# Kernel tuning notes

Measured on AMD Instinct MI355X. Metric: run time of the kernel, lower is better.

## Reference

```python
import jax, jax.numpy as jnp
import numpy as np

B, N, DE, DH, L, DC = 8, 256, 768, 192, 2, 192
NEG = 1e30  # mask_logic constant from the repo


def setup_inputs() -> dict:
    ks = iter(jax.random.split(jax.random.key(0), 32))

    def nrm(shape, s=0.02):
        return jax.random.normal(next(ks), shape, dtype=jnp.float32) * s

    features = jax.random.normal(next(ks), (B, N, DE), dtype=jnp.float32)
    # DAG adjacency: node i attends to a subset of j < i; guarantee edge (i, i-1)
    rnd = jax.random.bernoulli(next(ks), 0.3, (B, N, N))
    tril = jnp.tril(jnp.ones((N, N), jnp.bool_), -1)
    adj = ((rnd & tril[None]) | jnp.eye(N, k=-1, dtype=jnp.bool_)[None]).astype(jnp.float32)
    s_mask = jax.random.bernoulli(next(ks), 0.5, (B, N, N)).astype(jnp.float32)
    s_mask_onehot = jnp.stack([1.0 - s_mask, s_mask], axis=-1)  # unused in forward
    lengths = jnp.full((B,), N, dtype=jnp.int32)  # unused (nodal_att_type=None)
    return dict(
        features=features, adj=adj, s_mask=s_mask,
        s_mask_onehot=s_mask_onehot, lengths=lengths,
        fc1_w=nrm((DE, DH)), fc1_b=jnp.zeros((DH,), jnp.float32),
        gat_w=nrm((L, 2 * DH)), gat_b=jnp.zeros((L,), jnp.float32),
        wr0=nrm((L, DH, DH)), wr1=nrm((L, DH, DH)),
        gruc_wih=nrm((L, 3 * DH, DH)), gruc_whh=nrm((L, 3 * DH, DH)),
        gruc_bih=jnp.zeros((L, 3 * DH), jnp.float32),
        gruc_bhh=jnp.zeros((L, 3 * DH), jnp.float32),
        grup_wih=nrm((L, 3 * DH, DH)), grup_whh=nrm((L, 3 * DH, DH)),
        grup_bih=jnp.zeros((L, 3 * DH), jnp.float32),
        grup_bhh=jnp.zeros((L, 3 * DH), jnp.float32),
        mlp_w0=nrm((DH * (L + 1), DH)), mlp_b0=jnp.zeros((DH,), jnp.float32),
        mlp_w1=nrm((DH, DH)), mlp_b1=jnp.zeros((DH,), jnp.float32),
        mlp_w2=nrm((DH, DC)), mlp_b2=jnp.zeros((DC,), jnp.float32),
    )


def _gru(x, h, wih, whh, bih, bhh):
    # torch.nn.GRUCell math
    gi = x @ wih.T + bih
    gh = h @ whh.T + bhh
    ir, iz, inn = jnp.split(gi, 3, axis=-1)
    hr, hz, hn = jnp.split(gh, 3, axis=-1)
    r = jax.nn.sigmoid(ir + hr)
    z = jax.nn.sigmoid(iz + hz)
    n = jnp.tanh(inn + r * hn)
    return (1.0 - z) * n + z * h


def _layer(Hl, adj, s_mask, gat_w, gat_b, wr0, wr1, cw, cp):
    # One DAG layer: sequential scan over nodes. Carry holds the relation-
    # projected value buffers V0=H1@Wr0^T, V1=H1@Wr1^T and per-node key
    # scores Ksc=H1@wk (rows >= i are zero and masked out), which is
    # mathematically identical to the torch code that re-projects the
    # growing H1 every step.
    wq, wk = gat_w[:DH], gat_w[DH:]
    pos = jnp.arange(N)

    def step(carry, xs):
        V0, V1, Ksc = carry
        i, x_i, adj_i, sm_i = xs  # x_i:(B,DH) adj_i,sm_i:(B,N)
        score = (x_i @ wq)[:, None] + Ksc + gat_b          # (B,N)
        mask = (pos < i)[None, :] & (adj_i > 0.5)          # ragged :i slice
        alpha = jnp.where(mask, score, score - NEG)        # mask_logic
        attn = jax.nn.softmax(alpha, axis=-1)              # masked -> exactly 0
        Vrel = V0 * sm_i[..., None] + V1 * (1.0 - sm_i[..., None])
        M = jnp.einsum('bn,bnd->bd', attn, Vrel)
        M = jnp.where(i > 0, M, 0.0)                       # node 0: no context
        C = _gru(x_i, M, *cw)
        P = _gru(M, x_i, *cp)
        Hnew = C + P
        V0 = V0.at[:, i, :].set(Hnew @ wr0.T)
        V1 = V1.at[:, i, :].set(Hnew @ wr1.T)
        Ksc = Ksc.at[:, i].set(Hnew @ wk)
        attn_out = jnp.where(i > 0, attn, 0.0)             # adjB row 0 is zeros
        return (V0, V1, Ksc), (Hnew, attn_out)

    z3 = jnp.zeros((B, N, DH), jnp.float32)
    carry0 = (z3, z3, jnp.zeros((B, N), jnp.float32))
    xs = (pos, Hl.transpose(1, 0, 2), adj.transpose(1, 0, 2), s_mask.transpose(1, 0, 2))
    _, (Hseq, Aseq) = jax.lax.scan(step, carry0, xs)
    return Hseq.transpose(1, 0, 2), Aseq.transpose(1, 0, 2)  # (B,N,DH),(B,N,N)


def reference(features, adj, s_mask, s_mask_onehot, lengths,
              fc1_w, fc1_b, gat_w, gat_b, wr0, wr1,
              gruc_wih, gruc_whh, gruc_bih, gruc_bhh,
              grup_wih, grup_whh, grup_bih, grup_bhh,
              mlp_w0, mlp_b0, mlp_w1, mlp_b1, mlp_w2, mlp_b2):
    Hl = jax.nn.relu(features @ fc1_w + fc1_b)  # H0
    Hs, As = [Hl], []
    for l in range(L):
        cw = (gruc_wih[l], gruc_whh[l], gruc_bih[l], gruc_bhh[l])
        cp = (grup_wih[l], grup_whh[l], grup_bih[l], grup_bhh[l])
        Hl, Al = _layer(Hl, adj, s_mask, gat_w[l], gat_b[l], wr0[l], wr1[l], cw, cp)
        Hs.append(Hl)
        As.append(Al)
    H = jnp.concatenate(Hs, axis=2)  # (B,N,DH*(L+1))
    # nodal_att_type=None => attentive_node_features is identity
    h = jax.nn.relu(H @ mlp_w0 + mlp_b0)
    h = jax.nn.relu(h @ mlp_w1 + mlp_b1)  # mlp_layers-1 = 1 extra block
    logits = h @ mlp_w2 + mlp_b2          # dropout: eval-mode identity
    return logits, jnp.stack(As, axis=1)  # (B,N,DC), (B,L,N,N)
```

## Files before the change

kernel.cpp:

```cpp
#include <hip/hip_runtime.h>
#include <stdint.h>

#define B_  8
#define N_  256
#define DH_ 192
#define L_  2
#define G3  576
#define G6  1152
#define NW  4
#define DS  48
#define KD  24
#define GC  288
#define STH 10001
#define STP 20001
#define STQ 25001
#define SPK 50000
#define SF1 50001
#define SF2 50002
#define SDN 60001

typedef unsigned long long u64;

__device__ __forceinline__ float bflo(uint32_t u) { return __uint_as_float(u << 16); }
__device__ __forceinline__ float bfhi(uint32_t u) { return __uint_as_float(u & 0xffff0000u); }
__device__ __forceinline__ uint32_t f2bf(float f) {
    uint32_t x = __float_as_uint(f);
    x += 0x7fffu + ((x >> 16) & 1u);
    return x >> 16;
}
__device__ __forceinline__ float sigm(float x)  { return 1.f / (1.f + __expf(-x)); }
__device__ __forceinline__ float tanhf_(float x){ return 1.f - 2.f / (1.f + __expf(2.f * x)); }
__device__ __forceinline__ u64 packvs(float v, int st) {
    return ((u64)(uint32_t)st << 32) | __float_as_uint(v);
}
__device__ __forceinline__ u64 agload(const u64* p) {
    return __hip_atomic_load(p, __ATOMIC_RELAXED, __HIP_MEMORY_SCOPE_AGENT);
}
__device__ __forceinline__ void agstore(u64* p, u64 v) {
    __hip_atomic_store(p, v, __ATOMIC_RELAXED, __HIP_MEMORY_SCOPE_AGENT);
}

struct ScanSm {
    uint4 Wlds4[24 * GC];
    uint4 Wr4s[12 * DH_];
    float sA0[N_], sA1[N_], sKsc[N_];
    float sAdjN[N_], sSmN[N_];
    float sXq[DH_], sPre[6 * DS], sXv[DS];
    float sM[DH_], su0[DS], su1[DS], sGc[GC], sHn[DS];
    float sRedS[4], sRedX[3], sSaved[4];
};
struct WorkSm {
    uint4 Wp4[24 * GC];
    float sX[DH_];
    float sPv[GC];
    float sRed[3];
};
struct PrologSm {
    float sA[8][768];
    float sRed[3][8][192];
};
struct MlpSm {
    float sH[8][576];
    float sRed[3][8][192];
    float sT[8][192];
};

__device__ void prepack_slice(int idx,
    const float* __restrict__ wr0, const float* __restrict__ wr1,
    const float* __restrict__ c_wih, const float* __restrict__ c_whh,
    const float* __restrict__ c_bih, const float* __restrict__ c_bhh,
    const float* __restrict__ p_wih, const float* __restrict__ p_whh,
    const float* __restrict__ p_bih, const float* __restrict__ p_bhh,
    float* __restrict__ WpreT, uint32_t* __restrict__ W4,
    uint32_t* __restrict__ Wr4, uint32_t* __restrict__ Wp4w,
    float* __restrict__ biasPre, float* __restrict__ gbx)
{
    for (int l = 0; l < L_; ++l) {
        const float* cwih = c_wih + l * G3 * DH_;
        const float* cwhh = c_whh + l * G3 * DH_;
        const float* pwih = p_wih + l * G3 * DH_;
        const float* pwhh = p_whh + l * G3 * DH_;
        if (l == 0) {
            int k = idx / G6, r = idx - k * G6;
            float w = (r < G3) ? cwih[r * DH_ + k] : pwhh[(r - G3) * DH_ + k];
            WpreT[k * G6 + r] = w;
        }
        if (idx < NW * 27648) {
            int w = idx / 27648, pos = idx % 27648;
            int p4 = pos / 1152, rem = pos % 1152;
            int c2 = rem >> 2, s = rem & 3;
            int p = 4 * p4 + s;
            int j = c2 / DS, dd = c2 % DS;
            int c = 192 * j + DS * w + dd;
            float w0 = (c < G3) ? cwhh[c * DH_ + 2 * p]     : pwih[(c - G3) * DH_ + 2 * p];
            float w1 = (c < G3) ? cwhh[c * DH_ + 2 * p + 1] : pwih[(c - G3) * DH_ + 2 * p + 1];
            W4[l * NW * 27648 + idx] = f2bf(w0) | (f2bf(w1) << 16);
            if (l == 1) {
                int r = c;
                float v0 = (r < G3) ? cwih[r * DH_ + 2 * p]     : pwhh[(r - G3) * DH_ + 2 * p];
                float v1 = (r < G3) ? cwih[r * DH_ + 2 * p + 1] : pwhh[(r - G3) * DH_ + 2 * p + 1];
                Wp4w[idx] = f2bf(v0) | (f2bf(v1) << 16);
            }
        }
        if (idx < NW * 9216) {
            int w = idx / 9216, pos = idx % 9216;
            int kq = pos / 768, rem = pos % 768;
            int d = rem >> 2, s = rem & 3;
            int k = DS * w + 4 * kq + s;
            Wr4[l * NW * 9216 + idx] =
                f2bf(wr0[l * DH_ * DH_ + d * DH_ + k]) |
                (f2bf(wr1[l * DH_ * DH_ + d * DH_ + k]) << 16);
        }
        if (idx < G6) {
            float base = (idx < G3) ? c_bih[l * G3 + idx] : p_bhh[l * G3 + idx - G3];
            float fold = 0.f;
            if (idx < 384)                    fold = c_bhh[l * G3 + idx];
            else if (idx >= G3 && idx < 960)  fold = p_bih[l * G3 + idx - G3];
            biasPre[l * G6 + idx] = base + fold;
        }
        if (idx < 384) {
            gbx[l * 384 + idx] = (idx < DH_) ? c_bhh[l * G3 + 384 + idx]
                                             : p_bih[l * G3 + 384 + (idx - DH_)];
        }
    }
}

__device__ void flag_sync(u64* flags, int wgid, int t, int stamp)
{
    __threadfence();
    __syncthreads();
    if (t == 0) agstore(&flags[wgid], packvs(0.f, stamp));
    if (t < 96) {
        while ((uint32_t)(agload(&flags[t]) >> 32) != (uint32_t)stamp) {}
    }
    __syncthreads();
    __threadfence();
    __syncthreads();
}

__device__ void prologue(char* smem, int wgid, int t,
    const float* __restrict__ features, const float* __restrict__ fc1_w,
    const float* __restrict__ fc1_b, const float* __restrict__ WpreT,
    const float* __restrict__ biasPre,
    float* __restrict__ Hcat, float* __restrict__ PREg, u64* __restrict__ Fp)
{
    PrologSm* P = (PrologSm*)smem;
    const int c = t % 192, kg = t / 192;
    for (int tt = wgid; tt < 256; tt += 96) {
        const int r0 = tt * 8;
        for (int q = t; q < 1536; q += 576) {
            int r = q / 192, c4 = q % 192;
            *(float4*)&P->sA[r][4 * c4] = *(const float4*)(features + (size_t)(r0 + r) * 768 + 4 * c4);
        }
        __syncthreads();
        {
            const float* bp = fc1_w + (size_t)(kg * 256) * 192 + c;
            float acc[8] = {0.f, 0.f, 0.f, 0.f, 0.f, 0.f, 0.f, 0.f};
            #pragma unroll 8
            for (int kk = 0; kk < 256; ++kk) {
                float bv = bp[(size_t)kk * 192];
                #pragma unroll
                for (int rr = 0; rr < 8; ++rr) acc[rr] += P->sA[rr][kg * 256 + kk] * bv;
            }
            #pragma unroll
            for (int rr = 0; rr < 8; ++rr) P->sRed[kg][rr][c] = acc[rr];
        }
        __syncthreads();
        if (t < 192) {
            float bv = fc1_b[t];
            #pragma unroll
            for (int rr = 0; rr < 8; ++rr) {
                float v = P->sRed[0][rr][t] + P->sRed[1][rr][t] + P->sRed[2][rr][t] + bv;
                Hcat[(size_t)(r0 + rr) * G3 + t] = fmaxf(v, 0.f);
            }
        }
        __syncthreads();
    }
    flag_sync(Fp + 96, wgid, t, SF1);
    {
        const float bpa = biasPre[t], bpb = biasPre[576 + t];
        for (int tt = wgid; tt < 256; tt += 96) {
            const int r0 = tt * 8;
            for (int q = t; q < 384; q += 576) {
                int r = q / 48, c4 = q % 48;
                *(float4*)&P->sA[r][4 * c4] = *(const float4*)(Hcat + (size_t)(r0 + r) * G3 + 4 * c4);
            }
            __syncthreads();
            {
                const float* b0 = WpreT + t;
                float a0[8] = {0.f,0.f,0.f,0.f,0.f,0.f,0.f,0.f};
                float a1[8] = {0.f,0.f,0.f,0.f,0.f,0.f,0.f,0.f};
                #pragma unroll 4
                for (int k = 0; k < 192; ++k) {
                    float bva = b0[(size_t)k * G6];
                    float bvb = b0[(size_t)k * G6 + 576];
                    #pragma unroll
                    for (int rr = 0; rr < 8; ++rr) {
                        float av = P->sA[rr][k];
                        a0[rr] += av * bva; a1[rr] += av * bvb;
                    }
                }
                #pragma unroll
                for (int rr = 0; rr < 8; ++rr) {
                    PREg[(size_t)(r0 + rr) * G6 + t]       = a0[rr] + bpa;
                    PREg[(size_t)(r0 + rr) * G6 + 576 + t] = a1[rr] + bpb;
                }
            }
            __syncthreads();
        }
    }
    flag_sync(Fp + 192, wgid, t, SF2);
}

__device__ void mlp_tail(char* smem, int wgid, int t,
    const float* __restrict__ Hcat,
    const float* __restrict__ mw0, const float* __restrict__ mb0,
    const float* __restrict__ mw1, const float* __restrict__ mb1,
    const float* __restrict__ mw2, const float* __restrict__ mb2,
    float* __restrict__ out, u64* __restrict__ Fd)
{
    if (t < 64) {
        while ((uint32_t)(agload(&Fd[t]) >> 32) != (uint32_t)SDN) {}
    }
    __syncthreads();
    __threadfence();
    __syncthreads();
    MlpSm* M = (MlpSm*)smem;
    const int c = t % 192, kg = t / 192;
    for (int tt = wgid; tt < 256; tt += 96) {
        const int r0 = tt * 8;
        for (int q = t; q < 1152; q += 576) {
            int r = q / 144, c4 = q % 144;
            *(float4*)&M->sH[r][4 * c4] = *(const float4*)(Hcat + (size_t)(r0 + r) * G3 + 4 * c4);
        }
        __syncthreads();
        {
            const float* bp = mw0 + (size_t)(kg * 192) * 192 + c;
            float acc[8] = {0.f,0.f,0.f,0.f,0.f,0.f,0.f,0.f};
            #pragma unroll 8
            for (int kk = 0; kk < 192; ++kk) {
                float bv = bp[(size_t)kk * 192];
                #pragma unroll
                for (int rr = 0; rr < 8; ++rr) acc[rr] += M->sH[rr][kg * 192 + kk] * bv;
            }
            #pragma unroll
            for (int rr = 0; rr < 8; ++rr) M->sRed[kg][rr][c] = acc[rr];
        }
        __syncthreads();
        if (t < 192) {
            float bv = mb0[t];
            #pragma unroll
            for (int rr = 0; rr < 8; ++rr)
                M->sT[rr][t] = fmaxf(M->sRed[0][rr][t] + M->sRed[1][rr][t] + M->sRed[2][rr][t] + bv, 0.f);
        }
        __syncthreads();
        {
            const float* bp = mw1 + (size_t)(kg * 64) * 192 + c;
            float acc[8] = {0.f,0.f,0.f,0.f,0.f,0.f,0.f,0.f};
            #pragma unroll 8
            for (int kk = 0; kk < 64; ++kk) {
                float bv = bp[(size_t)kk * 192];
                #pragma unroll
                for (int rr = 0; rr < 8; ++rr) acc[rr] += M->sT[rr][kg * 64 + kk] * bv;
            }
            #pragma unroll
            for (int rr = 0; rr < 8; ++rr) M->sRed[kg][rr][c] = acc[rr];
        }
        __syncthreads();
        if (t < 192) {
            float bv = mb1[t];
            #pragma unroll
            for (int rr = 0; rr < 8; ++rr)
                M->sH[rr][t] = fmaxf(M->sRed[0][rr][t] + M->sRed[1][rr][t] + M->sRed[2][rr][t] + bv, 0.f);
        }
        __syncthreads();
        {
            const float* bp = mw2 + (size_t)(kg * 64) * 192 + c;
            float acc[8] = {0.f,0.f,0.f,0.f,0.f,0.f,0.f,0.f};
            #pragma unroll 8
            for (int kk = 0; kk < 64; ++kk) {
                float bv = bp[(size_t)kk * 192];
                #pragma unroll
                for (int rr = 0; rr < 8; ++rr) acc[rr] += M->sH[rr][kg * 64 + kk] * bv;
            }
            #pragma unroll
            for (int rr = 0; rr < 8; ++rr) M->sRed[kg][rr][c] = acc[rr];
        }
        __syncthreads();
        if (t < 192) {
            float bv = mb2[t];
            #pragma unroll
            for (int rr = 0; rr < 8; ++rr)
                out[(size_t)(r0 + rr) * 192 + t] =
                    M->sRed[0][rr][t] + M->sRed[1][rr][t] + M->sRed[2][rr][t] + bv;
        }
        __syncthreads();
    }
}

template<int ISL2>
__device__ void scan_body(
    ScanSm* S, int b, int w, int t,
    const float* __restrict__ xin, float* __restrict__ hout,
    const float* __restrict__ PREg, const float* __restrict__ adj,
    const float* __restrict__ smask,
    const uint32_t* __restrict__ W4l, const uint32_t* __restrict__ Wr4l,
    const float* __restrict__ gbxl, const float* __restrict__ gatwl,
    uint32_t* __restrict__ Hw, u64* __restrict__ MPsl, u64* __restrict__ Kdl,
    u64* __restrict__ HcW, const u64* __restrict__ HcR,
    const u64* __restrict__ PREcR, const u64* __restrict__ XQcR,
    float* __restrict__ AsB, int sbase)
{
    const int lane = t & 63, wave = t >> 6;
    const int dg0 = w * DS;
    const float* adjB = adj   + (size_t)b * N_ * N_;
    const float* smB  = smask + (size_t)b * N_ * N_;
    const int fi = b * NW;

    {
        uint32_t* wl = (uint32_t*)S->Wlds4;
        for (int q = t; q < 27648; q += 576) wl[q] = W4l[q];
        uint32_t* wr = (uint32_t*)S->Wr4s;
        for (int q = t; q < 9216; q += 576) wr[q] = Wr4l[q];
    }
    float wqv = (!ISL2 && t < DH_) ? gatwl[t] : 0.f;
    float wkv = 0.f, g2b = 0.f, g5b = 0.f;
    if (t < DS) { wkv = gatwl[DH_ + dg0 + t]; g2b = gbxl[dg0 + t]; g5b = gbxl[DH_ + dg0 + t]; }
    if (t < N_) S->sKsc[t] = 0.f;
    if (w == 0 && t < N_) AsB[t] = 0.f;

    if (!ISL2) {
        if (t < DS) {
            const float* pre = PREg + (size_t)(b * N_) * G6 + dg0 + t;
            S->sPre[t] = pre[0]; S->sPre[DS + t] = pre[192]; S->sPre[2 * DS + t] = pre[384];
            S->sPre[3 * DS + t] = pre[576]; S->sPre[4 * DS + t] = pre[768]; S->sPre[5 * DS + t] = pre[960];
            S->sXv[t] = xin[(size_t)(b * N_) * G3 + dg0 + t];
        }
        for (int q = t; q < 176; q += 576) {
            if (q < 64)       *(float4*)&S->sAdjN[4 * q] = *(const float4*)(adjB + N_ + 4 * q);
            else if (q < 128) { int q2 = q - 64;  *(float4*)&S->sSmN[4 * q2] = *(const float4*)(smB + N_ + 4 * q2); }
            else              { int q2 = q - 128; *(float4*)&S->sXq[4 * q2] = *(const float4*)(xin + (size_t)(b * N_ + 1) * G3 + 4 * q2); }
        }
    } else {
        for (int q = t; q < 321; q += 576) {
            if (q < 64)       *(float4*)&S->sAdjN[4 * q] = *(const float4*)(adjB + N_ + 4 * q);
            else if (q < 128) { int q2 = q - 64;  *(float4*)&S->sSmN[4 * q2] = *(const float4*)(smB + N_ + 4 * q2); }
            else if (q < 176) {
                int d = q - 128;
                const u64* p = HcR + ((size_t)(b * N_) * NW + w) * DS + d;
                u64 v; do { v = agload(p); } while ((uint32_t)(v >> 32) != (uint32_t)STH);
                S->sXv[d] = __uint_as_float((uint32_t)v);
            } else if (q < 320) {
                int qq = q - 176;
                const u64* p = PREcR + ((size_t)(b * N_) * NW + w) * 144 + qq;
                u64 v; do { v = agload(p); } while ((uint32_t)(v >> 32) != (uint32_t)STP);
                uint32_t pl = (uint32_t)v;
                S->sPre[2 * qq] = bflo(pl); S->sPre[2 * qq + 1] = bfhi(pl);
            } else {
                const u64* p = XQcR + b * N_ + 1;
                u64 v; do { v = agload(p); } while ((uint32_t)(v >> 32) != (uint32_t)(STQ + 1));
                S->sSaved[3] = __uint_as_float((uint32_t)v);
            }
        }
    }
    __syncthreads();
    {
        float hn = 0.f;
        if (t < DS) {
            float xv = S->sXv[t];
            float r1 = sigm(S->sPre[t]), z1 = sigm(S->sPre[DS + t]);
            float n1 = tanhf_(S->sPre[2 * DS + t] + r1 * g2b);
            float Cv = (1.f - z1) * n1;
            float r2 = sigm(S->sPre[3 * DS + t]), z2 = sigm(S->sPre[4 * DS + t]);
            float n2 = tanhf_(g5b + r2 * S->sPre[5 * DS + t]);
            hn = Cv + (1.f - z2) * n2 + z2 * xv;
            S->sHn[t] = hn;
            hout[(size_t)(b * N_) * G3 + dg0 + t] = hn;
            if (!ISL2) HcW[((size_t)(b * N_) * NW + w) * DS + t] = packvs(hn, STH);
        }
        if (wave == 0) {
            float v = hn * wkv;
            #pragma unroll
            for (int o = 32; o; o >>= 1) v += __shfl_xor(v, o);
            if (lane == 0) agstore(&Kdl[fi + w], packvs(v, sbase));
        }
    }
    __syncthreads();
    if (t < KD) Hw[(size_t)t * N_] = f2bf(S->sHn[2 * t]) | (f2bf(S->sHn[2 * t + 1]) << 16);
    if (!ISL2) {
        float px = (t < DH_) ? S->sXq[t] * wqv : 0.f;
        #pragma unroll
        for (int o = 32; o; o >>= 1) px += __shfl_xor(px, o);
        if (t < DH_ && lane == 0) S->sRedX[wave] = px;
    }
    __syncthreads();
    float xq = ISL2 ? S->sSaved[3] : (S->sRedX[0] + S->sRedX[1] + S->sRedX[2]);

    for (int i = 1; i < N_; ++i) {
        const int row = b * N_ + i;
        const int stamp = sbase + i;
        {
            float e = 0.f;
            if (t == i - 1) { S->sSaved[0] = S->sAdjN[t]; S->sSaved[1] = S->sSmN[t]; }
            if (t < N_) {
                if (t < i - 1 && S->sAdjN[t] > 0.5f) e = __expf(xq + S->sKsc[t]);
                float b0 = e * S->sSmN[t];
                S->sA0[t] = b0; S->sA1[t] = e - b0;
            }
            float ps = e;
            #pragma unroll
            for (int o = 32; o; o >>= 1) ps += __shfl_xor(ps, o);
            if (t < N_ && lane == 0) S->sRedS[wave] = ps;
        }
        __syncthreads();
        if (t < 384) {
            const int ilim = i - 1;
            const int kd = t >> 4, jp = t & 15;
            const uint32_t* hp = Hw + (size_t)kd * N_;
            float u0l = 0.f, u0h = 0.f, u1l = 0.f, u1h = 0.f;
            int j = jp;
            while (j + 48 < ilim) {
                uint32_t h0 = hp[j], h1 = hp[j + 16], h2 = hp[j + 32], h3 = hp[j + 48];
                float b0, b1;
                b0 = S->sA0[j];      b1 = S->sA1[j];
                u0l = fmaf(b0, bflo(h0), u0l); u0h = fmaf(b0, bfhi(h0), u0h);
                u1l = fmaf(b1, bflo(h0), u1l); u1h = fmaf(b1, bfhi(h0), u1h);
                b0 = S->sA0[j + 16]; b1 = S->sA1[j + 16];
                u0l = fmaf(b0, bflo(h1), u0l); u0h = fmaf(b0, bfhi(h1), u0h);
                u1l = fmaf(b1, bflo(h1), u1l); u1h = fmaf(b1, bfhi(h1), u1h);
                b0 = S->sA0[j + 32]; b1 = S->sA1[j + 32];
                u0l = fmaf(b0, bflo(h2), u0l); u0h = fmaf(b0, bfhi(h2), u0h);
                u1l = fmaf(b1, bflo(h2), u1l); u1h = fmaf(b1, bfhi(h2), u1h);
                b0 = S->sA0[j + 48]; b1 = S->sA1[j + 48];
                u0l = fmaf(b0, bflo(h3), u0l); u0h = fmaf(b0, bfhi(h3), u0h);
                u1l = fmaf(b1, bflo(h3), u1l); u1h = fmaf(b1, bfhi(h3), u1h);
                j += 64;
            }
            for (; j < ilim; j += 16) {
                uint32_t hv = hp[j];
                float b0 = S->sA0[j], b1 = S->sA1[j];
                u0l = fmaf(b0, bflo(hv), u0l); u0h = fmaf(b0, bfhi(hv), u0h);
                u1l = fmaf(b1, bflo(hv), u1l); u1h = fmaf(b1, bfhi(hv), u1h);
            }
            #pragma unroll
            for (int o = 1; o <= 8; o <<= 1) {
                u0l += __shfl_xor(u0l, o); u0h += __shfl_xor(u0h, o);
                u1l += __shfl_xor(u1l, o); u1h += __shfl_xor(u1h, o);
            }
            if (jp == 0) {
                S->su0[2 * kd] = u0l; S->su0[2 * kd + 1] = u0h;
                S->su1[2 * kd] = u1l; S->su1[2 * kd + 1] = u1h;
            }
        } else {
            const int u = t - 384;
            const int inx = (i + 1 < N_) ? i + 1 : N_ - 1;
            if (!ISL2) {
                for (int q = u; q < 260; q += 192) {
                    if (q < 64)
                        *(float4*)&S->sAdjN[4 * q] = *(const float4*)(adjB + (size_t)inx * N_ + 4 * q);
                    else if (q < 128) { int q2 = q - 64;
                        *(float4*)&S->sSmN[4 * q2] = *(const float4*)(smB + (size_t)inx * N_ + 4 * q2); }
                    else if (q < 140) { int q2 = q - 128;
                        *(float4*)&S->sXv[4 * q2] = *(const float4*)(xin + (size_t)row * G3 + dg0 + 4 * q2); }
                    else if (q < 212) { int q2 = q - 140; int g = q2 / 12, o = q2 - 12 * g;
                        *(float4*)&S->sPre[g * DS + 4 * o] =
                            *(const float4*)(PREg + (size_t)row * G6 + g * DH_ + dg0 + 4 * o); }
                    else { int q2 = q - 212;
                        *(float4*)&S->sXq[4 * q2] = *(const float4*)(xin + (size_t)(b * N_ + inx) * G3 + 4 * q2); }
                }
            } else {
                for (int q = u; q < 321; q += 192) {
                    if (q < 64)
                        *(float4*)&S->sAdjN[4 * q] = *(const float4*)(adjB + (size_t)inx * N_ + 4 * q);
                    else if (q < 128) { int q2 = q - 64;
                        *(float4*)&S->sSmN[4 * q2] = *(const float4*)(smB + (size_t)inx * N_ + 4 * q2); }
                    else if (q < 176) {
                        int d = q - 128;
                        const u64* p = HcR + ((size_t)row * NW + w) * DS + d;
                        u64 v; do { v = agload(p); } while ((uint32_t)(v >> 32) != (uint32_t)(STH + i));
                        S->sXv[d] = __uint_as_float((uint32_t)v);
                    } else if (q < 320) {
                        int qq = q - 176;
                        const u64* p = PREcR + ((size_t)row * NW + w) * 144 + qq;
                        u64 v; do { v = agload(p); } while ((uint32_t)(v >> 32) != (uint32_t)(STP + i));
                        uint32_t pl = (uint32_t)v;
                        S->sPre[2 * qq] = bflo(pl); S->sPre[2 * qq + 1] = bfhi(pl);
                    } else {
                        const u64* p = XQcR + b * N_ + inx;
                        u64 v; do { v = agload(p); } while ((uint32_t)(v >> 32) != (uint32_t)(STQ + inx));
                        S->sSaved[3] = __uint_as_float((uint32_t)v);
                    }
                }
            }
            if (t == 575) {
                const uint32_t ex = (uint32_t)(stamp - 1);
                u64 k0, k1, k2, k3;
                do {
                    k0 = agload(&Kdl[fi + 0]); k1 = agload(&Kdl[fi + 1]);
                    k2 = agload(&Kdl[fi + 2]); k3 = agload(&Kdl[fi + 3]);
                } while ((uint32_t)(k0 >> 32) != ex || (uint32_t)(k1 >> 32) != ex ||
                         (uint32_t)(k2 >> 32) != ex || (uint32_t)(k3 >> 32) != ex);
                float kdot = __uint_as_float((uint32_t)k0) + __uint_as_float((uint32_t)k1)
                           + __uint_as_float((uint32_t)k2) + __uint_as_float((uint32_t)k3);
                float adjI1 = S->sSaved[0], smI1 = S->sSaved[1];
                float e1 = (adjI1 > 0.5f) ? __expf(xq + kdot) : 0.f;
                float Ssum = S->sRedS[0] + S->sRedS[1] + S->sRedS[2] + S->sRedS[3] + e1;
                S->sKsc[i - 1] = kdot;
                float c0 = e1 * smI1;
                S->sA0[i - 1] = c0; S->sA1[i - 1] = e1 - c0;
                S->sSaved[2] = 1.f / Ssum;
            }
        }
        __syncthreads();
        if (t < DH_) {
            float mp = 0.f, h0a = 0.f, h1a = 0.f;
            #pragma unroll 4
            for (int kq = 0; kq < 12; ++kq) {
                uint4 wv = S->Wr4s[kq * DH_ + t];
                const int k0 = 4 * kq;
                float lo, hi;
                lo = bflo(wv.x); hi = bfhi(wv.x);
                mp = fmaf(S->su0[k0 + 0], lo, mp); mp = fmaf(S->su1[k0 + 0], hi, mp);
                h0a = fmaf(S->sHn[k0 + 0], lo, h0a); h1a = fmaf(S->sHn[k0 + 0], hi, h1a);
                lo = bflo(wv.y); hi = bfhi(wv.y);
                mp = fmaf(S->su0[k0 + 1], lo, mp); mp = fmaf(S->su1[k0 + 1], hi, mp);
                h0a = fmaf(S->sHn[k0 + 1], lo, h0a); h1a = fmaf(S->sHn[k0 + 1], hi, h1a);
                lo = bflo(wv.z); hi = bfhi(wv.z);
                mp = fmaf(S->su0[k0 + 2], lo, mp); mp = fmaf(S->su1[k0 + 2], hi, mp);
                h0a = fmaf(S->sHn[k0 + 2], lo, h0a); h1a = fmaf(S->sHn[k0 + 2], hi, h1a);
                lo = bflo(wv.w); hi = bfhi(wv.w);
                mp = fmaf(S->su0[k0 + 3], lo, mp); mp = fmaf(S->su1[k0 + 3], hi, mp);
                h0a = fmaf(S->sHn[k0 + 3], lo, h0a); h1a = fmaf(S->sHn[k0 + 3], hi, h1a);
            }
            float invS = S->sSaved[2];
            mp = (mp + S->sA0[i - 1] * h0a + S->sA1[i - 1] * h1a) * invS;
            agstore(&MPsl[(size_t)(fi + w) * DH_ + t], packvs(mp, stamp));
            const int w1 = (w + 1) & 3, w2 = (w + 2) & 3, w3 = (w + 3) & 3;
            u64* pA = &MPsl[(size_t)(fi + w1) * DH_ + t];
            u64* pB = &MPsl[(size_t)(fi + w2) * DH_ + t];
            u64* pC = &MPsl[(size_t)(fi + w3) * DH_ + t];
            const uint32_t ex = (uint32_t)stamp;
            u64 vA, vB, vC;
            do {
                vA = agload(pA); vB = agload(pB); vC = agload(pC);
            } while ((uint32_t)(vA >> 32) != ex || (uint32_t)(vB >> 32) != ex ||
                     (uint32_t)(vC >> 32) != ex);
            S->sM[t] = mp + __uint_as_float((uint32_t)vA)
                          + __uint_as_float((uint32_t)vB)
                          + __uint_as_float((uint32_t)vC);
        } else if (w == 0 && t < 448) {
            int j = t - 192;
            AsB[(size_t)i * N_ + j] = (S->sA0[j] + S->sA1[j]) * S->sSaved[2];
        }
        __syncthreads();
        {
            const int c = t >> 1, kh = t & 1;
            const uint4* wp = S->Wlds4 + (12 * kh) * GC + c;
            float g = 0.f;
            #pragma unroll 4
            for (int p4 = 0; p4 < 12; ++p4) {
                uint4 wv = wp[p4 * GC];
                const int m0 = 8 * (12 * kh + p4);
                g = fmaf(S->sM[m0 + 0], bflo(wv.x), g); g = fmaf(S->sM[m0 + 1], bfhi(wv.x), g);
                g = fmaf(S->sM[m0 + 2], bflo(wv.y), g); g = fmaf(S->sM[m0 + 3], bfhi(wv.y), g);
                g = fmaf(S->sM[m0 + 4], bflo(wv.z), g); g = fmaf(S->sM[m0 + 5], bfhi(wv.z), g);
                g = fmaf(S->sM[m0 + 6], bflo(wv.w), g); g = fmaf(S->sM[m0 + 7], bfhi(wv.w), g);
            }
            g += __shfl_xor(g, 1);
            if (kh == 0) S->sGc[c] = g;
        }
        __syncthreads();
        {
            float hn = 0.f;
            if (t < DS) {
                float Mv = S->sM[dg0 + t];
                float r1 = sigm(S->sPre[t] + S->sGc[t]);
                float z1 = sigm(S->sPre[DS + t] + S->sGc[DS + t]);
                float n1 = tanhf_(S->sPre[2 * DS + t] + r1 * (S->sGc[2 * DS + t] + g2b));
                float Cv = (1.f - z1) * n1 + z1 * Mv;
                float r2 = sigm(S->sGc[3 * DS + t] + S->sPre[3 * DS + t]);
                float z2 = sigm(S->sGc[4 * DS + t] + S->sPre[4 * DS + t]);
                float n2 = tanhf_(S->sGc[5 * DS + t] + g5b + r2 * S->sPre[5 * DS + t]);
                hn = Cv + (1.f - z2) * n2 + z2 * S->sXv[t];
                S->sHn[t] = hn;
                hout[(size_t)row * G3 + dg0 + t] = hn;
                if (!ISL2) HcW[((size_t)row * NW + w) * DS + t] = packvs(hn, STH + i);
            }
            if (wave == 0) {
                float v = hn * wkv;
                #pragma unroll
                for (int o = 32; o; o >>= 1) v += __shfl_xor(v, o);
                if (lane == 0) agstore(&Kdl[fi + w], packvs(v, stamp));
            }
            if (t < KD) Hw[(size_t)t * N_ + i] = f2bf(S->sHn[2 * t]) | (f2bf(S->sHn[2 * t + 1]) << 16);
            if (!ISL2) {
                float px = (t < DH_) ? S->sXq[t] * wqv : 0.f;
                #pragma unroll
                for (int o = 32; o; o >>= 1) px += __shfl_xor(px, o);
                if (t < DH_ && lane == 0) S->sRedX[wave] = px;
            }
        }
        __syncthreads();
        xq = ISL2 ? S->sSaved[3] : (S->sRedX[0] + S->sRedX[1] + S->sRedX[2]);
    }
}

__device__ void worker_body(WorkSm* Wm, int b, int w, int t,
    const uint32_t* __restrict__ Wp4g, const float* __restrict__ bias2,
    const float* __restrict__ wq2,
    const u64* __restrict__ HcR, u64* __restrict__ PREcW, u64* __restrict__ XQcW)
{
    const int lane = t & 63, wave = t >> 6;
    { uint32_t* wl = (uint32_t*)Wm->Wp4; for (int q = t; q < 27648; q += 576) wl[q] = Wp4g[q]; }
    const int c = t >> 1, kh = t & 1;
    float bv = 0.f;
    if (kh == 0) bv = bias2[192 * (c / DS) + w * DS + (c % DS)];
    float wqt = (t < DH_) ? wq2[t] : 0.f;
    for (int i = 0; i < N_; ++i) {
        if (t < DH_) {
            const u64* p = HcR + ((size_t)(b * N_ + i) * NW + (t / DS)) * DS + (t % DS);
            u64 v; do { v = agload(p); } while ((uint32_t)(v >> 32) != (uint32_t)(STH + i));
            Wm->sX[t] = __uint_as_float((uint32_t)v);
        }
        __syncthreads();
        {
            const uint4* wp = Wm->Wp4 + (12 * kh) * GC + c;
            float g = 0.f;
            #pragma unroll 4
            for (int p4 = 0; p4 < 12; ++p4) {
                uint4 wv = wp[p4 * GC];
                const int m0 = 8 * (12 * kh + p4);
                g = fmaf(Wm->sX[m0 + 0], bflo(wv.x), g); g = fmaf(Wm->sX[m0 + 1], bfhi(wv.x), g);
                g = fmaf(Wm->sX[m0 + 2], bflo(wv.y), g); g = fmaf(Wm->sX[m0 + 3], bfhi(wv.y), g);
                g = fmaf(Wm->sX[m0 + 4], bflo(wv.z), g); g = fmaf(Wm->sX[m0 + 5], bfhi(wv.z), g);
                g = fmaf(Wm->sX[m0 + 6], bflo(wv.w), g); g = fmaf(Wm->sX[m0 + 7], bfhi(wv.w), g);
            }
            g += __shfl_xor(g, 1);
            if (kh == 0) Wm->sPv[c] = g + bv;
        }
        if (w == 0) {
            float px = (t < DH_) ? Wm->sX[t] * wqt : 0.f;
            #pragma unroll
            for (int o = 32; o; o >>= 1) px += __shfl_xor(px, o);
            if (t < DH_ && lane == 0) Wm->sRed[wave] = px;
        }
        __syncthreads();
        if (t < 144) {
            u64 v = ((u64)(uint32_t)(STP + i) << 32)
                  | f2bf(Wm->sPv[2 * t]) | (f2bf(Wm->sPv[2 * t + 1]) << 16);
            agstore(&PREcW[((size_t)(b * N_ + i) * NW + w) * 144 + t], v);
        }
        if (w == 0 && t == 0)
            agstore(&XQcW[b * N_ + i],
                    packvs(Wm->sRed[0] + Wm->sRed[1] + Wm->sRed[2], STQ + i));
        __syncthreads();
    }
}

__global__ __launch_bounds__(576, 1) void pipeline_kernel(
    const float* __restrict__ features, const float* __restrict__ fc1_w,
    const float* __restrict__ fc1_b,
    const float* __restrict__ adj, const float* __restrict__ smask,
    const float* __restrict__ gatw,
    const float* __restrict__ wr0, const float* __restrict__ wr1,
    const float* __restrict__ c_wih, const float* __restrict__ c_whh,
    const float* __restrict__ c_bih, const float* __restrict__ c_bhh,
    const float* __restrict__ p_wih, const float* __restrict__ p_whh,
    const float* __restrict__ p_bih, const float* __restrict__ p_bhh,
    const float* __restrict__ mw0, const float* __restrict__ mb0,
    const float* __restrict__ mw1, const float* __restrict__ mb1,
    const float* __restrict__ mw2, const float* __restrict__ mb2,
    float* __restrict__ Hcat, float* __restrict__ PREg,
    float* __restrict__ WpreT, uint32_t* __restrict__ W4,
    uint32_t* __restrict__ Wr4, uint32_t* __restrict__ Wp4w,
    float* __restrict__ biasPre, float* __restrict__ gbx,
    uint32_t* __restrict__ Hb, u64* __restrict__ MPs, u64* __restrict__ Kd,
    u64* __restrict__ Hc, u64* __restrict__ PREc, u64* __restrict__ XQc,
    u64* __restrict__ Fp, u64* __restrict__ Fd,
    float* __restrict__ out)
{
    __shared__ __align__(16) char smem[sizeof(ScanSm)];
    const int blk = blockIdx.x, t = threadIdx.x;
    const int wgid = blk;
    const int b = blk & 7, r12 = blk >> 3;
    const int role = r12 >> 2, w = r12 & 3;

    for (int j = 0; j < 4; ++j) {
        int idx = wgid * 576 + t + 55296 * j;
        prepack_slice(idx, wr0, wr1, c_wih, c_whh, c_bih, c_bhh,
                      p_wih, p_whh, p_bih, p_bhh,
                      WpreT, W4, Wr4, Wp4w, biasPre, gbx);
    }
    flag_sync(Fp, wgid, t, SPK);

    prologue(smem, wgid, t, features, fc1_w, fc1_b, WpreT, biasPre,
             Hcat, PREg, Fp);

    float* As = out + 393216;
    if (role == 0) {
        scan_body<0>((ScanSm*)smem, b, w, t,
            Hcat, Hcat + 192, PREg, adj, smask,
            W4, Wr4, gbx, gatw,
            Hb + (size_t)(b * NW + w) * KD * N_, MPs, Kd,
            Hc, nullptr, nullptr, nullptr,
            As + (size_t)b * (L_ * N_ * N_), 1);
        __threadfence();
        __syncthreads();
        if (t == 0) agstore(&Fd[b * 8 + w], packvs(0.f, SDN));
    } else if (role == 2) {
        scan_body<1>((ScanSm*)smem, b, w, t,
            nullptr, Hcat + 384, nullptr, adj, smask,
            W4 + NW * 27648, Wr4 + NW * 9216, gbx + 384, gatw + 384,
            Hb + (size_t)(32 + b * NW + w) * KD * N_,
            MPs + (size_t)8 * NW * DH_, Kd + 8 * NW,
            nullptr, Hc, PREc, XQc,
            As + (size_t)b * (L_ * N_ * N_) + N_ * N_, 30001);
        __threadfence();
        __syncthreads();
        if (t == 0) agstore(&Fd[b * 8 + 4 + w], packvs(0.f, SDN));
    } else {
        worker_body((WorkSm*)smem, b, w, t,
            Wp4w + (size_t)w * 27648, biasPre + G6, gatw + 384,
            Hc, PREc, XQc);
    }

    mlp_tail(smem, wgid, t, Hcat, mw0, mb0, mw1, mb1, mw2, mb2, out, Fd);
}

extern "C" void kernel_launch(void* const* d_in, const int* in_sizes, int n_in,
                              void* d_out, int out_size, void* d_ws, size_t ws_size,
                              hipStream_t stream)
{
    const float* features = (const float*)d_in[0];
    const float* adj      = (const float*)d_in[1];
    const float* smask    = (const float*)d_in[2];
    const float* fc1_w = (const float*)d_in[5];
    const float* fc1_b = (const float*)d_in[6];
    const float* gat_w = (const float*)d_in[7];
    const float* wr0   = (const float*)d_in[9];
    const float* wr1   = (const float*)d_in[10];
    const float* c_wih = (const float*)d_in[11];
    const float* c_whh = (const float*)d_in[12];
    const float* c_bih = (const float*)d_in[13];
    const float* c_bhh = (const float*)d_in[14];
    const float* p_wih = (const float*)d_in[15];
    const float* p_whh = (const float*)d_in[16];
    const float* p_bih = (const float*)d_in[17];
    const float* p_bhh = (const float*)d_in[18];
    const float* mw0 = (const float*)d_in[19];
    const float* mb0 = (const float*)d_in[20];
    const float* mw1 = (const float*)d_in[21];
    const float* mb1 = (const float*)d_in[22];
    const float* mw2 = (const float*)d_in[23];
    const float* mb2 = (const float*)d_in[24];
    float* out = (float*)d_out;

    char* wsb = (char*)d_ws;
    size_t off = 0;
    auto carve = [&](size_t bytes) -> char* {
        char* p = wsb + off;
        off = (off + bytes + 255) & ~(size_t)255;
        return p;
    };
    float* Hcat     = (float*)carve(2048ull * 576 * 4);
    float* PREg     = (float*)carve(2048ull * 1152 * 4);
    float* WpreT    = (float*)carve(192ull * 1152 * 4);
    uint32_t* W4    = (uint32_t*)carve(2ull * NW * 27648 * 4);
    uint32_t* Wr4   = (uint32_t*)carve(2ull * NW * 9216 * 4);
    uint32_t* Wp4w  = (uint32_t*)carve((size_t)NW * 27648 * 4);
    float* biasPre  = (float*)carve(2ull * 1152 * 4);
    float* gbx      = (float*)carve(2ull * 384 * 4);
    uint32_t* Hb    = (uint32_t*)carve(64ull * KD * 256 * 4);
    u64* MPs        = (u64*)carve(2ull * 8 * NW * DH_ * 8);
    u64* Kd         = (u64*)carve(2ull * 8 * NW * 8);
    u64* Hc         = (u64*)carve(8ull * 256 * NW * DS * 8);
    u64* PREc       = (u64*)carve(8ull * 256 * NW * 144 * 8);
    u64* XQc        = (u64*)carve(8ull * 256 * 8);
    u64* Fp         = (u64*)carve(288ull * 8);
    u64* Fd         = (u64*)carve(64ull * 8);

    pipeline_kernel<<<dim3(96), 576, 0, stream>>>(
        features, fc1_w, fc1_b, adj, smask, gat_w,
        wr0, wr1, c_wih, c_whh, c_bih, c_bhh, p_wih, p_whh, p_bih, p_bhh,
        mw0, mb0, mw1, mb1, mw2, mb2,
        Hcat, PREg, WpreT, W4, Wr4, Wp4w, biasPre, gbx,
        Hb, MPs, Kd, Hc, PREc, XQc, Fp, Fd, out);
}
```

Baseline: 1.915 ms.

## Run each batch's scan in one workgroup instead of four cross-CU slices

```diff
diff --git a/kernel.cpp b/kernel.cpp
--- a/kernel.cpp
+++ b/kernel.cpp
@@ -1,19 +1,12 @@
 #include <hip/hip_runtime.h>
 #include <stdint.h>
 
-#define B_  8
 #define N_  256
 #define DH_ 192
-#define L_  2
 #define G3  576
 #define G6  1152
-#define NW  4
-#define DS  48
-#define KD  24
-#define GC  288
 #define STH 10001
 #define STP 20001
-#define STQ 25001
 #define SPK 50000
 #define SF1 50001
 #define SF2 50002
@@ -39,22 +32,25 @@
 __device__ __forceinline__ void agstore(u64* p, u64 v) {
     __hip_atomic_store(p, v, __ATOMIC_RELAXED, __HIP_MEMORY_SCOPE_AGENT);
 }
+__device__ __forceinline__ float u2f(u64 v) { return __uint_as_float((uint32_t)v); }
 
 struct ScanSm {
-    uint4 Wlds4[24 * GC];
-    uint4 Wr4s[12 * DH_];
-    float sA0[N_], sA1[N_], sKsc[N_];
-    float sAdjN[N_], sSmN[N_];
-    float sXq[DH_], sPre[6 * DS], sXv[DS];
-    float sM[DH_], su0[DS], su1[DS], sGc[GC], sHn[DS];
-    float sRedS[4], sRedX[3], sSaved[4];
+    uint32_t Hw[N_ * 96];
+    float sPre[2][G6];
+    float sXv[2][DH_];
+    float sAdj[2][N_];
+    float sSm[2][N_];
+    float sKsc[N_];
+    float sA0[N_], sA1[N_];
+    float sHn[DH_];
+    float sU0p[12][DH_], sU1p[12][DH_];
+    float sMp[3][DH_];
+    float sM[DH_];
+    float su0[DH_], su1[DH_];
+    float sGc[G6];
+    float sRedS[4], sRedK[4];
 };
-struct WorkSm {
-    uint4 Wp4[24 * GC];
-    float sX[DH_];
-    float sPv[GC];
-    float sRed[3];
-};
+struct WorkSm { float sX[DH_]; };
 struct PrologSm {
     float sA[8][768];
     float sRed[3][8][192];
@@ -64,64 +60,49 @@
     float sRed[3][8][192];
     float sT[8][192];
 };
+union SmemAll { ScanSm s; WorkSm w; PrologSm p; MlpSm m; };
 
 __device__ void prepack_slice(int idx,
-    const float* __restrict__ wr0, const float* __restrict__ wr1,
     const float* __restrict__ c_wih, const float* __restrict__ c_whh,
     const float* __restrict__ c_bih, const float* __restrict__ c_bhh,
     const float* __restrict__ p_wih, const float* __restrict__ p_whh,
     const float* __restrict__ p_bih, const float* __restrict__ p_bhh,
-    float* __restrict__ WpreT, uint32_t* __restrict__ W4,
-    uint32_t* __restrict__ Wr4, uint32_t* __restrict__ Wp4w,
-    float* __restrict__ biasPre, float* __restrict__ gbx)
-{
-    for (int l = 0; l < L_; ++l) {
-        const float* cwih = c_wih + l * G3 * DH_;
-        const float* cwhh = c_whh + l * G3 * DH_;
-        const float* pwih = p_wih + l * G3 * DH_;
-        const float* pwhh = p_whh + l * G3 * DH_;
-        if (l == 0) {
-            int k = idx / G6, r = idx - k * G6;
-            float w = (r < G3) ? cwih[r * DH_ + k] : pwhh[(r - G3) * DH_ + k];
-            WpreT[k * G6 + r] = w;
-        }
-        if (idx < NW * 27648) {
-            int w = idx / 27648, pos = idx % 27648;
-            int p4 = pos / 1152, rem = pos % 1152;
-            int c2 = rem >> 2, s = rem & 3;
-            int p = 4 * p4 + s;
-            int j = c2 / DS, dd = c2 % DS;
-            int c = 192 * j + DS * w + dd;
-            float w0 = (c < G3) ? cwhh[c * DH_ + 2 * p]     : pwih[(c - G3) * DH_ + 2 * p];
-            float w1 = (c < G3) ? cwhh[c * DH_ + 2 * p + 1] : pwih[(c - G3) * DH_ + 2 * p + 1];
-            W4[l * NW * 27648 + idx] = f2bf(w0) | (f2bf(w1) << 16);
-            if (l == 1) {
-                int r = c;
-                float v0 = (r < G3) ? cwih[r * DH_ + 2 * p]     : pwhh[(r - G3) * DH_ + 2 * p];
-                float v1 = (r < G3) ? cwih[r * DH_ + 2 * p + 1] : pwhh[(r - G3) * DH_ + 2 * p + 1];
-                Wp4w[idx] = f2bf(v0) | (f2bf(v1) << 16);
-            }
-        }
-        if (idx < NW * 9216) {
-            int w = idx / 9216, pos = idx % 9216;
-            int kq = pos / 768, rem = pos % 768;
-            int d = rem >> 2, s = rem & 3;
-            int k = DS * w + 4 * kq + s;
-            Wr4[l * NW * 9216 + idx] =
-                f2bf(wr0[l * DH_ * DH_ + d * DH_ + k]) |
-                (f2bf(wr1[l * DH_ * DH_ + d * DH_ + k]) << 16);
-        }
-        if (idx < G6) {
-            float base = (idx < G3) ? c_bih[l * G3 + idx] : p_bhh[l * G3 + idx - G3];
-            float fold = 0.f;
-            if (idx < 384)                    fold = c_bhh[l * G3 + idx];
-            else if (idx >= G3 && idx < 960)  fold = p_bih[l * G3 + idx - G3];
-            biasPre[l * G6 + idx] = base + fold;
-        }
-        if (idx < 384) {
-            gbx[l * 384 + idx] = (idx < DH_) ? c_bhh[l * G3 + 384 + idx]
-                                             : p_bih[l * G3 + 384 + (idx - DH_)];
-        }
+    float* __restrict__ WpreT, uint32_t* __restrict__ Wc,
+    uint32_t* __restrict__ Wp, float* __restrict__ biasPre,
+    float* __restrict__ gbx)
+{
+    {
+        int k = idx / G6, r = idx - k * G6;
+        float w = (r < G3) ? c_wih[r * DH_ + k] : p_whh[(r - G3) * DH_ + k];
+        WpreT[k * G6 + r] = w;
+    }
+    {
+        int l = idx / 110592, o = idx - l * 110592;
+        int k4 = o / 2304, r3 = o - k4 * 2304, cp = r3 >> 2, kk = r3 & 3;
+        int k = 4 * k4 + kk, c0 = 2 * cp;
+        const float* W = (c0 < G3) ? (c_whh + (size_t)(l * G3 + c0) * DH_)
+                                   : (p_wih + (size_t)(l * G3 + c0 - G3) * DH_);
+        Wc[idx] = f2bf(W[k]) | (f2bf(W[DH_ + k]) << 16);
+    }
+    if (idx < 110592) {
+        int k4 = idx / 2304, r3 = idx - k4 * 2304, cp = r3 >> 2, kk = r3 & 3;
+        int k = 4 * k4 + kk, c0 = 2 * cp;
+        const float* W = (c0 < G3) ? (c_wih + (size_t)(G3 + c0) * DH_)
+                                   : (p_whh + (size_t)(G3 + c0 - G3) * DH_);
+        Wp[idx] = f2bf(W[k]) | (f2bf(W[DH_ + k]) << 16);
+    }
+    if (idx < 2304) {
+        int l = idx / G6, c = idx - l * G6;
+        float base = (c < G3) ? c_bih[l * G3 + c] : p_bhh[l * G3 + c - G3];
+        float fold = 0.f;
+        if (c < 384)                   fold = c_bhh[l * G3 + c];
+        else if (c >= G3 && c < 960)   fold = p_bih[l * G3 + c - G3];
+        biasPre[idx] = base + fold;
+    }
+    if (idx < 768) {
+        int l = idx / 384, c = idx - l * 384;
+        gbx[idx] = (c < DH_) ? c_bhh[l * G3 + 384 + c]
+                             : p_bih[l * G3 + 384 + (c - DH_)];
     }
 }
 
@@ -219,8 +200,9 @@
     const float* __restrict__ mw2, const float* __restrict__ mb2,
     float* __restrict__ out, u64* __restrict__ Fd)
 {
-    if (t < 64) {
-        while ((uint32_t)(agload(&Fd[t]) >> 32) != (uint32_t)SDN) {}
+    if (t < 16) {
+        while ((uint32_t)(agload(&Fd[t]) >> 32) != (uint32_t)SDN)
+            __builtin_amdgcn_s_sleep(2);
     }
     __syncthreads();
     __threadfence();
@@ -299,360 +281,249 @@
 }
 
 template<int ISL2>
-__device__ void scan_body(
-    ScanSm* S, int b, int w, int t,
+__device__ void scan_full(ScanSm* S, int b, int t,
     const float* __restrict__ xin, float* __restrict__ hout,
-    const float* __restrict__ PREg, const float* __restrict__ adj,
-    const float* __restrict__ smask,
-    const uint32_t* __restrict__ W4l, const uint32_t* __restrict__ Wr4l,
-    const float* __restrict__ gbxl, const float* __restrict__ gatwl,
-    uint32_t* __restrict__ Hw, u64* __restrict__ MPsl, u64* __restrict__ Kdl,
+    const float* __restrict__ PREg,
+    const float* __restrict__ adj, const float* __restrict__ smask,
+    const uint32_t* __restrict__ Wc,
+    const float* __restrict__ wr0l, const float* __restrict__ wr1l,
+    const float* __restrict__ gbxl, const float* __restrict__ wkp,
     u64* __restrict__ HcW, const u64* __restrict__ HcR,
-    const u64* __restrict__ PREcR, const u64* __restrict__ XQcR,
-    float* __restrict__ AsB, int sbase)
+    const u64* __restrict__ PREcR,
+    float* __restrict__ AsB)
 {
     const int lane = t & 63, wave = t >> 6;
-    const int dg0 = w * DS;
     const float* adjB = adj   + (size_t)b * N_ * N_;
     const float* smB  = smask + (size_t)b * N_ * N_;
-    const int fi = b * NW;
-
-    {
-        uint32_t* wl = (uint32_t*)S->Wlds4;
-        for (int q = t; q < 27648; q += 576) wl[q] = W4l[q];
-        uint32_t* wr = (uint32_t*)S->Wr4s;
-        for (int q = t; q < 9216; q += 576) wr[q] = Wr4l[q];
-    }
-    float wqv = (!ISL2 && t < DH_) ? gatwl[t] : 0.f;
+    const int dM = t % DH_, kgM = t / DH_;
+    const int kpU = t % 48,  jgU = t / 48;
+
+    uint32_t wreg[64];
+    for (int kk = 0; kk < 64; ++kk) {
+        int k = kgM * 64 + kk;
+        wreg[kk] = f2bf(wr0l[dM * DH_ + k]) | (f2bf(wr1l[dM * DH_ + k]) << 16);
+    }
     float wkv = 0.f, g2b = 0.f, g5b = 0.f;
-    if (t < DS) { wkv = gatwl[DH_ + dg0 + t]; g2b = gbxl[dg0 + t]; g5b = gbxl[DH_ + dg0 + t]; }
-    if (t < N_) S->sKsc[t] = 0.f;
-    if (w == 0 && t < N_) AsB[t] = 0.f;
+    if (t < DH_) { wkv = wkp[t]; g2b = gbxl[t]; g5b = gbxl[DH_ + t]; }
+    if (t < N_) AsB[t] = 0.f;
 
     if (!ISL2) {
-        if (t < DS) {
-            const float* pre = PREg + (size_t)(b * N_) * G6 + dg0 + t;
-            S->sPre[t] = pre[0]; S->sPre[DS + t] = pre[192]; S->sPre[2 * DS + t] = pre[384];
-            S->sPre[3 * DS + t] = pre[576]; S->sPre[4 * DS + t] = pre[768]; S->sPre[5 * DS + t] = pre[960];
-            S->sXv[t] = xin[(size_t)(b * N_) * G3 + dg0 + t];
-        }
-        for (int q = t; q < 176; q += 576) {
-            if (q < 64)       *(float4*)&S->sAdjN[4 * q] = *(const float4*)(adjB + N_ + 4 * q);
-            else if (q < 128) { int q2 = q - 64;  *(float4*)&S->sSmN[4 * q2] = *(const float4*)(smB + N_ + 4 * q2); }
-            else              { int q2 = q - 128; *(float4*)&S->sXq[4 * q2] = *(const float4*)(xin + (size_t)(b * N_ + 1) * G3 + 4 * q2); }
+        for (int q = t; q < 800; q += 576) {
+            if (q < 288)      *(float4*)&S->sPre[0][4*q] = *(const float4*)(PREg + (size_t)(b*N_)*G6 + 4*q);
+            else if (q < 336) { int q2=q-288; *(float4*)&S->sXv[0][4*q2] = *(const float4*)(xin + (size_t)(b*N_)*G3 + 4*q2); }
+            else if (q < 624) { int q2=q-336; *(float4*)&S->sPre[1][4*q2] = *(const float4*)(PREg + (size_t)(b*N_+1)*G6 + 4*q2); }
+            else if (q < 672) { int q2=q-624; *(float4*)&S->sXv[1][4*q2] = *(const float4*)(xin + (size_t)(b*N_+1)*G3 + 4*q2); }
+            else if (q < 736) { int q2=q-672; *(float4*)&S->sAdj[1][4*q2] = *(const float4*)(adjB + N_ + 4*q2); }
+            else              { int q2=q-736; *(float4*)&S->sSm[1][4*q2] = *(const float4*)(smB + N_ + 4*q2); }
         }
     } else {
-        for (int q = t; q < 321; q += 576) {
-            if (q < 64)       *(float4*)&S->sAdjN[4 * q] = *(const float4*)(adjB + N_ + 4 * q);
-            else if (q < 128) { int q2 = q - 64;  *(float4*)&S->sSmN[4 * q2] = *(const float4*)(smB + N_ + 4 * q2); }
-            else if (q < 176) {
-                int d = q - 128;
-                const u64* p = HcR + ((size_t)(b * N_) * NW + w) * DS + d;
+        for (int q = t; q < 1664; q += 576) {
+            if (q < 192) {
+                const u64* p = HcR + (size_t)(b*N_)*DH_ + q;
                 u64 v; do { v = agload(p); } while ((uint32_t)(v >> 32) != (uint32_t)STH);
-                S->sXv[d] = __uint_as_float((uint32_t)v);
-            } else if (q < 320) {
-                int qq = q - 176;
-                const u64* p = PREcR + ((size_t)(b * N_) * NW + w) * 144 + qq;
+                S->sXv[0][q] = u2f(v);
+            } else if (q < 768) {
+                int idx = q - 192;
+                const u64* p = PREcR + (size_t)(b*N_)*G3 + idx;
                 u64 v; do { v = agload(p); } while ((uint32_t)(v >> 32) != (uint32_t)STP);
                 uint32_t pl = (uint32_t)v;
-                S->sPre[2 * qq] = bflo(pl); S->sPre[2 * qq + 1] = bfhi(pl);
-            } else {
-                const u64* p = XQcR + b * N_ + 1;
-                u64 v; do { v = agload(p); } while ((uint32_t)(v >> 32) != (uint32_t)(STQ + 1));
-                S->sSaved[3] = __uint_as_float((uint32_t)v);
-            }
+                S->sPre[0][2*idx] = bflo(pl); S->sPre[0][2*idx+1] = bfhi(pl);
+            } else if (q < 960) {
+                int d = q - 768;
+                const u64* p = HcR + (size_t)(b*N_+1)*DH_ + d;
+                u64 v; do { v = agload(p); } while ((uint32_t)(v >> 32) != (uint32_t)(STH+1));
+                S->sXv[1][d] = u2f(v);
+            } else if (q < 1536) {
+                int idx = q - 960;
+                const u64* p = PREcR + (size_t)(b*N_+1)*G3 + idx;
+                u64 v; do { v = agload(p); } while ((uint32_t)(v >> 32) != (uint32_t)(STP+1));
+                uint32_t pl = (uint32_t)v;
+                S->sPre[1][2*idx] = bflo(pl); S->sPre[1][2*idx+1] = bfhi(pl);
+            } else if (q < 1600) { int q2 = q-1536; *(float4*)&S->sAdj[1][4*q2] = *(const float4*)(adjB + N_ + 4*q2); }
+            else                 { int q2 = q-1600; *(float4*)&S->sSm[1][4*q2]  = *(const float4*)(smB  + N_ + 4*q2); }
         }
     }
     __syncthreads();
-    {
-        float hn = 0.f;
-        if (t < DS) {
-            float xv = S->sXv[t];
-            float r1 = sigm(S->sPre[t]), z1 = sigm(S->sPre[DS + t]);
-            float n1 = tanhf_(S->sPre[2 * DS + t] + r1 * g2b);
-            float Cv = (1.f - z1) * n1;
-            float r2 = sigm(S->sPre[3 * DS + t]), z2 = sigm(S->sPre[4 * DS + t]);
-            float n2 = tanhf_(g5b + r2 * S->sPre[5 * DS + t]);
-            hn = Cv + (1.f - z2) * n2 + z2 * xv;
-            S->sHn[t] = hn;
-            hout[(size_t)(b * N_) * G3 + dg0 + t] = hn;
-            if (!ISL2) HcW[((size_t)(b * N_) * NW + w) * DS + t] = packvs(hn, STH);
-        }
-        if (wave == 0) {
-            float v = hn * wkv;
-            #pragma unroll
-            for (int o = 32; o; o >>= 1) v += __shfl_xor(v, o);
-            if (lane == 0) agstore(&Kdl[fi + w], packvs(v, sbase));
-        }
-    }
-    __syncthreads();
-    if (t < KD) Hw[(size_t)t * N_] = f2bf(S->sHn[2 * t]) | (f2bf(S->sHn[2 * t + 1]) << 16);
-    if (!ISL2) {
-        float px = (t < DH_) ? S->sXq[t] * wqv : 0.f;
+
+    if (t < DH_) {
+        const float* Pr = S->sPre[0];
+        float xv = S->sXv[0][t];
+        float r1 = sigm(Pr[t]), z1 = sigm(Pr[DH_ + t]);
+        float n1 = tanhf_(Pr[2*DH_ + t] + r1 * g2b);
+        float Cv = (1.f - z1) * n1;
+        float r2 = sigm(Pr[3*DH_ + t]), z2 = sigm(Pr[4*DH_ + t]);
+        float n2 = tanhf_(g5b + r2 * Pr[5*DH_ + t]);
+        float hn = Cv + (1.f - z2) * n2 + z2 * xv;
+        S->sHn[t] = hn;
+        hout[(size_t)(b*N_)*G3 + t] = hn;
+        if (!ISL2) agstore(&HcW[(size_t)(b*N_)*DH_ + t], packvs(hn, STH));
+        float px = hn * wkv;
         #pragma unroll
         for (int o = 32; o; o >>= 1) px += __shfl_xor(px, o);
-        if (t < DH_ && lane == 0) S->sRedX[wave] = px;
+        if (lane == 0) S->sRedK[wave] = px;
     }
     __syncthreads();
-    float xq = ISL2 ? S->sSaved[3] : (S->sRedX[0] + S->sRedX[1] + S->sRedX[2]);
 
     for (int i = 1; i < N_; ++i) {
-        const int row = b * N_ + i;
-        const int stamp = sbase + i;
-        {
-            float e = 0.f;
-            if (t == i - 1) { S->sSaved[0] = S->sAdjN[t]; S->sSaved[1] = S->sSmN[t]; }
-            if (t < N_) {
-                if (t < i - 1 && S->sAdjN[t] > 0.5f) e = __expf(xq + S->sKsc[t]);
-                float b0 = e * S->sSmN[t];
-                S->sA0[t] = b0; S->sA1[t] = e - b0;
-            }
+        const int row = b*N_ + i;
+        const int pp = i & 1, pn = pp ^ 1;
+        const int inx = (i + 1 < N_) ? i + 1 : N_ - 1;
+
+        if (t < N_) {
+            float ksc;
+            if (t == i - 1) { ksc = S->sRedK[0] + S->sRedK[1] + S->sRedK[2]; S->sKsc[i-1] = ksc; }
+            else            ksc = S->sKsc[t];
+            float e = (t < i && S->sAdj[pp][t] > 0.5f) ? __expf(ksc) : 0.f;
+            float a0 = e * S->sSm[pp][t];
+            S->sA0[t] = a0; S->sA1[t] = e - a0;
             float ps = e;
             #pragma unroll
             for (int o = 32; o; o >>= 1) ps += __shfl_xor(ps, o);
-            if (t < N_ && lane == 0) S->sRedS[wave] = ps;
-        }
-        __syncthreads();
-        if (t < 384) {
-            const int ilim = i - 1;
-            const int kd = t >> 4, jp = t & 15;
-            const uint32_t* hp = Hw + (size_t)kd * N_;
-            float u0l = 0.f, u0h = 0.f, u1l = 0.f, u1h = 0.f;
-            int j = jp;
-            while (j + 48 < ilim) {
-                uint32_t h0 = hp[j], h1 = hp[j + 16], h2 = hp[j + 32], h3 = hp[j + 48];
-                float b0, b1;
-                b0 = S->sA0[j];      b1 = S->sA1[j];
-                u0l = fmaf(b0, bflo(h0), u0l); u0h = fmaf(b0, bfhi(h0), u0h);
-                u1l = fmaf(b1, bflo(h0), u1l); u1h = fmaf(b1, bfhi(h0), u1h);
-                b0 = S->sA0[j + 16]; b1 = S->sA1[j + 16];
-                u0l = fmaf(b0, bflo(h1), u0l); u0h = fmaf(b0, bfhi(h1), u0h);
-                u1l = fmaf(b1, bflo(h1), u1l); u1h = fmaf(b1, bfhi(h1), u1h);
-                b0 = S->sA0[j + 32]; b1 = S->sA1[j + 32];
-                u0l = fmaf(b0, bflo(h2), u0l); u0h = fmaf(b0, bfhi(h2), u0h);
-                u1l = fmaf(b1, bflo(h2), u1l); u1h = fmaf(b1, bfhi(h2), u1h);
-                b0 = S->sA0[j + 48]; b1 = S->sA1[j + 48];
-                u0l = fmaf(b0, bflo(h3), u0l); u0h = fmaf(b0, bfhi(h3), u0h);
-                u1l = fmaf(b1, bflo(h3), u1l); u1h = fmaf(b1, bfhi(h3), u1h);
-                j += 64;
-            }
-            for (; j < ilim; j += 16) {
-                uint32_t hv = hp[j];
-                float b0 = S->sA0[j], b1 = S->sA1[j];
-                u0l = fmaf(b0, bflo(hv), u0l); u0h = fmaf(b0, bfhi(hv), u0h);
-                u1l = fmaf(b1, bflo(hv), u1l); u1h = fmaf(b1, bfhi(hv), u1h);
-            }
-            #pragma unroll
-            for (int o = 1; o <= 8; o <<= 1) {
-                u0l += __shfl_xor(u0l, o); u0h += __shfl_xor(u0h, o);
-                u1l += __shfl_xor(u1l, o); u1h += __shfl_xor(u1h, o);
-            }
-            if (jp == 0) {
-                S->su0[2 * kd] = u0l; S->su0[2 * kd + 1] = u0h;
-                S->su1[2 * kd] = u1l; S->su1[2 * kd + 1] = u1h;
-            }
+            if (lane == 0) S->sRedS[wave] = ps;
         } else {
-            const int u = t - 384;
-            const int inx = (i + 1 < N_) ? i + 1 : N_ - 1;
             if (!ISL2) {
-                for (int q = u; q < 260; q += 192) {
-                    if (q < 64)
-                        *(float4*)&S->sAdjN[4 * q] = *(const float4*)(adjB + (size_t)inx * N_ + 4 * q);
-                    else if (q < 128) { int q2 = q - 64;
-                        *(float4*)&S->sSmN[4 * q2] = *(const float4*)(smB + (size_t)inx * N_ + 4 * q2); }
-                    else if (q < 140) { int q2 = q - 128;
-                        *(float4*)&S->sXv[4 * q2] = *(const float4*)(xin + (size_t)row * G3 + dg0 + 4 * q2); }
-                    else if (q < 212) { int q2 = q - 140; int g = q2 / 12, o = q2 - 12 * g;
-                        *(float4*)&S->sPre[g * DS + 4 * o] =
-                            *(const float4*)(PREg + (size_t)row * G6 + g * DH_ + dg0 + 4 * o); }
-                    else { int q2 = q - 212;
-                        *(float4*)&S->sXq[4 * q2] = *(const float4*)(xin + (size_t)(b * N_ + inx) * G3 + 4 * q2); }
+                for (int q = t - 256; q < 560; q += 320) {
+                    if (q < 96) S->Hw[(i-1)*96 + q] = f2bf(S->sHn[2*q]) | (f2bf(S->sHn[2*q+1]) << 16);
+                    else {
+                        int j = q - 96;
+                        if (j < 64)       *(float4*)&S->sAdj[pn][4*j] = *(const float4*)(adjB + (size_t)inx*N_ + 4*j);
+                        else if (j < 128) { int j2=j-64;  *(float4*)&S->sSm[pn][4*j2]  = *(const float4*)(smB  + (size_t)inx*N_ + 4*j2); }
+                        else if (j < 176) { int j2=j-128; *(float4*)&S->sXv[pn][4*j2]  = *(const float4*)(xin  + (size_t)(b*N_+inx)*G3 + 4*j2); }
+                        else              { int j2=j-176; *(float4*)&S->sPre[pn][4*j2] = *(const float4*)(PREg + (size_t)(b*N_+inx)*G6 + 4*j2); }
+                    }
                 }
             } else {
-                for (int q = u; q < 321; q += 192) {
-                    if (q < 64)
-                        *(float4*)&S->sAdjN[4 * q] = *(const float4*)(adjB + (size_t)inx * N_ + 4 * q);
-                    else if (q < 128) { int q2 = q - 64;
-                        *(float4*)&S->sSmN[4 * q2] = *(const float4*)(smB + (size_t)inx * N_ + 4 * q2); }
-                    else if (q < 176) {
-                        int d = q - 128;
-                        const u64* p = HcR + ((size_t)row * NW + w) * DS + d;
-                        u64 v; do { v = agload(p); } while ((uint32_t)(v >> 32) != (uint32_t)(STH + i));
-                        S->sXv[d] = __uint_as_float((uint32_t)v);
-                    } else if (q < 320) {
-                        int qq = q - 176;
-                        const u64* p = PREcR + ((size_t)row * NW + w) * 144 + qq;
-                        u64 v; do { v = agload(p); } while ((uint32_t)(v >> 32) != (uint32_t)(STP + i));
+                for (int q = t - 256; q < 992; q += 320) {
+                    if (q < 96) S->Hw[(i-1)*96 + q] = f2bf(S->sHn[2*q]) | (f2bf(S->sHn[2*q+1]) << 16);
+                    else if (q < 160) { int j = q-96;  *(float4*)&S->sAdj[pn][4*j] = *(const float4*)(adjB + (size_t)inx*N_ + 4*j); }
+                    else if (q < 224) { int j = q-160; *(float4*)&S->sSm[pn][4*j]  = *(const float4*)(smB  + (size_t)inx*N_ + 4*j); }
+                    else if (q < 416) {
+                        int d = q - 224;
+                        const u64* p = HcR + (size_t)(b*N_+inx)*DH_ + d;
+                        u64 v; do { v = agload(p); } while ((uint32_t)(v >> 32) != (uint32_t)(STH+inx));
+                        S->sXv[pn][d] = u2f(v);
+                    } else {
+                        int idx = q - 416;
+                        const u64* p = PREcR + (size_t)(b*N_+inx)*G3 + idx;
+                        u64 v; do { v = agload(p); } while ((uint32_t)(v >> 32) != (uint32_t)(STP+inx));
                         uint32_t pl = (uint32_t)v;
-                        S->sPre[2 * qq] = bflo(pl); S->sPre[2 * qq + 1] = bfhi(pl);
-                    } else {
-                        const u64* p = XQcR + b * N_ + inx;
-                        u64 v; do { v = agload(p); } while ((uint32_t)(v >> 32) != (uint32_t)(STQ + inx));
-                        S->sSaved[3] = __uint_as_float((uint32_t)v);
+                        S->sPre[pn][2*idx] = bflo(pl); S->sPre[pn][2*idx+1] = bfhi(pl);
                     }
                 }
             }
-            if (t == 575) {
-                const uint32_t ex = (uint32_t)(stamp - 1);
-                u64 k0, k1, k2, k3;
-                do {
-                    k0 = agload(&Kdl[fi + 0]); k1 = agload(&Kdl[fi + 1]);
-                    k2 = agload(&Kdl[fi + 2]); k3 = agload(&Kdl[fi + 3]);
-                } while ((uint32_t)(k0 >> 32) != ex || (uint32_t)(k1 >> 32) != ex ||
-                         (uint32_t)(k2 >> 32) != ex || (uint32_t)(k3 >> 32) != ex);
-                float kdot = __uint_as_float((uint32_t)k0) + __uint_as_float((uint32_t)k1)
-                           + __uint_as_float((uint32_t)k2) + __uint_as_float((uint32_t)k3);
-                float adjI1 = S->sSaved[0], smI1 = S->sSaved[1];
-                float e1 = (adjI1 > 0.5f) ? __expf(xq + kdot) : 0.f;
-                float Ssum = S->sRedS[0] + S->sRedS[1] + S->sRedS[2] + S->sRedS[3] + e1;
-                S->sKsc[i - 1] = kdot;
-                float c0 = e1 * smI1;
-                S->sA0[i - 1] = c0; S->sA1[i - 1] = e1 - c0;
-                S->sSaved[2] = 1.f / Ssum;
-            }
-        }
-        __syncthreads();
+        }
+        __syncthreads();
+
+        {
+            float4 u0 = {0.f,0.f,0.f,0.f}, u1 = {0.f,0.f,0.f,0.f};
+            const int kb = 2 * kpU;
+            for (int j = jgU; j < i; j += 12) {
+                uint32_t h0 = S->Hw[j*96 + kb], h1 = S->Hw[j*96 + kb + 1];
+                float a0 = S->sA0[j], a1 = S->sA1[j];
+                u0.x += a0*bflo(h0); u0.y += a0*bfhi(h0);
+                u0.z += a0*bflo(h1); u0.w += a0*bfhi(h1);
+                u1.x += a1*bflo(h0); u1.y += a1*bfhi(h0);
+                u1.z += a1*bflo(h1); u1.w += a1*bfhi(h1);
+            }
+            *(float4*)&S->sU0p[jgU][4*kpU] = u0;
+            *(float4*)&S->sU1p[jgU][4*kpU] = u1;
+        }
+        __syncthreads();
+
+        {
+            float invS = 1.f / (S->sRedS[0] + S->sRedS[1] + S->sRedS[2] + S->sRedS[3]);
+            if (t < DH_) {
+                float v0 = 0.f, v1 = 0.f;
+                #pragma unroll
+                for (int g = 0; g < 12; ++g) { v0 += S->sU0p[g][t]; v1 += S->sU1p[g][t]; }
+                S->su0[t] = v0 * invS; S->su1[t] = v1 * invS;
+            } else if (t < DH_ + N_) {
+                int j = t - DH_;
+                AsB[(size_t)i*N_ + j] = (j < i) ? (S->sA0[j] + S->sA1[j]) * invS : 0.f;
+            }
+        }
+        __syncthreads();
+
+        {
+            float m = 0.f;
+            const float4* s0 = (const float4*)&S->su0[kgM * 64];
+            const float4* s1 = (const float4*)&S->su1[kgM * 64];
+            #pragma unroll
+            for (int k4 = 0; k4 < 16; ++k4) {
+                float4 a = s0[k4], c = s1[k4];
+                m += bflo(wreg[4*k4+0])*a.x + bfhi(wreg[4*k4+0])*c.x;
+                m += bflo(wreg[4*k4+1])*a.y + bfhi(wreg[4*k4+1])*c.y;
+                m += bflo(wreg[4*k4+2])*a.z + bfhi(wreg[4*k4+2])*c.z;
+                m += bflo(wreg[4*k4+3])*a.w + bfhi(wreg[4*k4+3])*c.w;
+            }
+            S->sMp[kgM][dM] = m;
+        }
+        __syncthreads();
+        if (t < DH_) S->sM[t] = S->sMp[0][t] + S->sMp[1][t] + S->sMp[2][t];
+        __syncthreads();
+
+        {
+            float g0 = 0.f, g1 = 0.f;
+            const uint4* wp4 = (const uint4*)Wc;
+            #pragma unroll 4
+            for (int k4 = 0; k4 < 48; ++k4) {
+                uint4 wv = wp4[k4*576 + t];
+                float4 mv = *(const float4*)&S->sM[4*k4];
+                g0 += bflo(wv.x)*mv.x + bflo(wv.y)*mv.y + bflo(wv.z)*mv.z + bflo(wv.w)*mv.w;
+                g1 += bfhi(wv.x)*mv.x + bfhi(wv.y)*mv.y + bfhi(wv.z)*mv.z + bfhi(wv.w)*mv.w;
+            }
+            S->sGc[2*t] = g0; S->sGc[2*t+1] = g1;
+        }
+        __syncthreads();
+
         if (t < DH_) {
-            float mp = 0.f, h0a = 0.f, h1a = 0.f;
-            #pragma unroll 4
-            for (int kq = 0; kq < 12; ++kq) {
-                uint4 wv = S->Wr4s[kq * DH_ + t];
-                const int k0 = 4 * kq;
-                float lo, hi;
-                lo = bflo(wv.x); hi = bfhi(wv.x);
-                mp = fmaf(S->su0[k0 + 0], lo, mp); mp = fmaf(S->su1[k0 + 0], hi, mp);
-                h0a = fmaf(S->sHn[k0 + 0], lo, h0a); h1a = fmaf(S->sHn[k0 + 0], hi, h1a);
-                lo = bflo(wv.y); hi = bfhi(wv.y);
-                mp = fmaf(S->su0[k0 + 1], lo, mp); mp = fmaf(S->su1[k0 + 1], hi, mp);
-                h0a = fmaf(S->sHn[k0 + 1], lo, h0a); h1a = fmaf(S->sHn[k0 + 1], hi, h1a);
-                lo = bflo(wv.z); hi = bfhi(wv.z);
-                mp = fmaf(S->su0[k0 + 2], lo, mp); mp = fmaf(S->su1[k0 + 2], hi, mp);
-                h0a = fmaf(S->sHn[k0 + 2], lo, h0a); h1a = fmaf(S->sHn[k0 + 2], hi, h1a);
-                lo = bflo(wv.w); hi = bfhi(wv.w);
-                mp = fmaf(S->su0[k0 + 3], lo, mp); mp = fmaf(S->su1[k0 + 3], hi, mp);
-                h0a = fmaf(S->sHn[k0 + 3], lo, h0a); h1a = fmaf(S->sHn[k0 + 3], hi, h1a);
-            }
-            float invS = S->sSaved[2];
-            mp = (mp + S->sA0[i - 1] * h0a + S->sA1[i - 1] * h1a) * invS;
-            agstore(&MPsl[(size_t)(fi + w) * DH_ + t], packvs(mp, stamp));
-            const int w1 = (w + 1) & 3, w2 = (w + 2) & 3, w3 = (w + 3) & 3;
-            u64* pA = &MPsl[(size_t)(fi + w1) * DH_ + t];
-            u64* pB = &MPsl[(size_t)(fi + w2) * DH_ + t];
-            u64* pC = &MPsl[(size_t)(fi + w3) * DH_ + t];
-            const uint32_t ex = (uint32_t)stamp;
-            u64 vA, vB, vC;
-            do {
-                vA = agload(pA); vB = agload(pB); vC = agload(pC);
-            } while ((uint32_t)(vA >> 32) != ex || (uint32_t)(vB >> 32) != ex ||
-                     (uint32_t)(vC >> 32) != ex);
-            S->sM[t] = mp + __uint_as_float((uint32_t)vA)
-                          + __uint_as_float((uint32_t)vB)
-                          + __uint_as_float((uint32_t)vC);
-        } else if (w == 0 && t < 448) {
-            int j = t - 192;
-            AsB[(size_t)i * N_ + j] = (S->sA0[j] + S->sA1[j]) * S->sSaved[2];
-        }
-        __syncthreads();
-        {
-            const int c = t >> 1, kh = t & 1;
-            const uint4* wp = S->Wlds4 + (12 * kh) * GC + c;
-            float g = 0.f;
-            #pragma unroll 4
-            for (int p4 = 0; p4 < 12; ++p4) {
-                uint4 wv = wp[p4 * GC];
-                const int m0 = 8 * (12 * kh + p4);
-                g = fmaf(S->sM[m0 + 0], bflo(wv.x), g); g = fmaf(S->sM[m0 + 1], bfhi(wv.x), g);
-                g = fmaf(S->sM[m0 + 2], bflo(wv.y), g); g = fmaf(S->sM[m0 + 3], bfhi(wv.y), g);
-                g = fmaf(S->sM[m0 + 4], bflo(wv.z), g); g = fmaf(S->sM[m0 + 5], bfhi(wv.z), g);
-                g = fmaf(S->sM[m0 + 6], bflo(wv.w), g); g = fmaf(S->sM[m0 + 7], bfhi(wv.w), g);
-            }
-            g += __shfl_xor(g, 1);
-            if (kh == 0) S->sGc[c] = g;
-        }
-        __syncthreads();
-        {
-            float hn = 0.f;
-            if (t < DS) {
-                float Mv = S->sM[dg0 + t];
-                float r1 = sigm(S->sPre[t] + S->sGc[t]);
-                float z1 = sigm(S->sPre[DS + t] + S->sGc[DS + t]);
-                float n1 = tanhf_(S->sPre[2 * DS + t] + r1 * (S->sGc[2 * DS + t] + g2b));
-                float Cv = (1.f - z1) * n1 + z1 * Mv;
-                float r2 = sigm(S->sGc[3 * DS + t] + S->sPre[3 * DS + t]);
-                float z2 = sigm(S->sGc[4 * DS + t] + S->sPre[4 * DS + t]);
-                float n2 = tanhf_(S->sGc[5 * DS + t] + g5b + r2 * S->sPre[5 * DS + t]);
-                hn = Cv + (1.f - z2) * n2 + z2 * S->sXv[t];
-                S->sHn[t] = hn;
-                hout[(size_t)row * G3 + dg0 + t] = hn;
-                if (!ISL2) HcW[((size_t)row * NW + w) * DS + t] = packvs(hn, STH + i);
-            }
-            if (wave == 0) {
-                float v = hn * wkv;
-                #pragma unroll
-                for (int o = 32; o; o >>= 1) v += __shfl_xor(v, o);
-                if (lane == 0) agstore(&Kdl[fi + w], packvs(v, stamp));
-            }
-            if (t < KD) Hw[(size_t)t * N_ + i] = f2bf(S->sHn[2 * t]) | (f2bf(S->sHn[2 * t + 1]) << 16);
-            if (!ISL2) {
-                float px = (t < DH_) ? S->sXq[t] * wqv : 0.f;
-                #pragma unroll
-                for (int o = 32; o; o >>= 1) px += __shfl_xor(px, o);
-                if (t < DH_ && lane == 0) S->sRedX[wave] = px;
-            }
-        }
-        __syncthreads();
-        xq = ISL2 ? S->sSaved[3] : (S->sRedX[0] + S->sRedX[1] + S->sRedX[2]);
-    }
-}
-
-__device__ void worker_body(WorkSm* Wm, int b, int w, int t,
-    const uint32_t* __restrict__ Wp4g, const float* __restrict__ bias2,
-    const float* __restrict__ wq2,
-    const u64* __restrict__ HcR, u64* __restrict__ PREcW, u64* __restrict__ XQcW)
-{
-    const int lane = t & 63, wave = t >> 6;
-    { uint32_t* wl = (uint32_t*)Wm->Wp4; for (int q = t; q < 27648; q += 576) wl[q] = Wp4g[q]; }
-    const int c = t >> 1, kh = t & 1;
-    float bv = 0.f;
-    if (kh == 0) bv = bias2[192 * (c / DS) + w * DS + (c % DS)];
-    float wqt = (t < DH_) ? wq2[t] : 0.f;
+            const float* Pr = S->sPre[pp];
+            const float* Gc = S->sGc;
+            float Mv = S->sM[t];
+            float r1 = sigm(Pr[t] + Gc[t]);
+            float z1 = sigm(Pr[DH_+t] + Gc[DH_+t]);
+            float n1 = tanhf_(Pr[2*DH_+t] + r1 * (Gc[2*DH_+t] + g2b));
+            float Cv = (1.f - z1) * n1 + z1 * Mv;
+            float r2 = sigm(Gc[3*DH_+t] + Pr[3*DH_+t]);
+            float z2 = sigm(Gc[4*DH_+t] + Pr[4*DH_+t]);
+            float n2 = tanhf_(Gc[5*DH_+t] + g5b + r2 * Pr[5*DH_+t]);
+            float hn = Cv + (1.f - z2) * n2 + z2 * S->sXv[pp][t];
+            S->sHn[t] = hn;
+            hout[(size_t)row*G3 + t] = hn;
+            if (!ISL2) agstore(&HcW[(size_t)row*DH_ + t], packvs(hn, STH + i));
+            float px = hn * wkv;
+            #pragma unroll
+            for (int o = 32; o; o >>= 1) px += __shfl_xor(px, o);
+            if (lane == 0) S->sRedK[wave] = px;
+        }
+        __syncthreads();
+    }
+}
+
+__device__ void worker_full(float* sX, int b, int t,
+    const uint32_t* __restrict__ Wp, const float* __restrict__ bias2,
+    const u64* __restrict__ HcR, u64* __restrict__ PREcW)
+{
+    const float bv0 = bias2[2*t], bv1 = bias2[2*t + 1];
+    const uint4* wp4 = (const uint4*)Wp;
     for (int i = 0; i < N_; ++i) {
         if (t < DH_) {
-            const u64* p = HcR + ((size_t)(b * N_ + i) * NW + (t / DS)) * DS + (t % DS);
+            const u64* p = HcR + (size_t)(b*N_ + i)*DH_ + t;
             u64 v; do { v = agload(p); } while ((uint32_t)(v >> 32) != (uint32_t)(STH + i));
-            Wm->sX[t] = __uint_as_float((uint32_t)v);
-        }
-        __syncthreads();
-        {
-            const uint4* wp = Wm->Wp4 + (12 * kh) * GC + c;
-            float g = 0.f;
-            #pragma unroll 4
-            for (int p4 = 0; p4 < 12; ++p4) {
-                uint4 wv = wp[p4 * GC];
-                const int m0 = 8 * (12 * kh + p4);
-                g = fmaf(Wm->sX[m0 + 0], bflo(wv.x), g); g = fmaf(Wm->sX[m0 + 1], bfhi(wv.x), g);
-                g = fmaf(Wm->sX[m0 + 2], bflo(wv.y), g); g = fmaf(Wm->sX[m0 + 3], bfhi(wv.y), g);
-                g = fmaf(Wm->sX[m0 + 4], bflo(wv.z), g); g = fmaf(Wm->sX[m0 + 5], bfhi(wv.z), g);
-                g = fmaf(Wm->sX[m0 + 6], bflo(wv.w), g); g = fmaf(Wm->sX[m0 + 7], bfhi(wv.w), g);
-            }
-            g += __shfl_xor(g, 1);
-            if (kh == 0) Wm->sPv[c] = g + bv;
-        }
-        if (w == 0) {
-            float px = (t < DH_) ? Wm->sX[t] * wqt : 0.f;
-            #pragma unroll
-            for (int o = 32; o; o >>= 1) px += __shfl_xor(px, o);
-            if (t < DH_ && lane == 0) Wm->sRed[wave] = px;
-        }
-        __syncthreads();
-        if (t < 144) {
-            u64 v = ((u64)(uint32_t)(STP + i) << 32)
-                  | f2bf(Wm->sPv[2 * t]) | (f2bf(Wm->sPv[2 * t + 1]) << 16);
-            agstore(&PREcW[((size_t)(b * N_ + i) * NW + w) * 144 + t], v);
-        }
-        if (w == 0 && t == 0)
-            agstore(&XQcW[b * N_ + i],
-                    packvs(Wm->sRed[0] + Wm->sRed[1] + Wm->sRed[2], STQ + i));
+            sX[t] = u2f(v);
+        }
+        __syncthreads();
+        float g0 = 0.f, g1 = 0.f;
+        #pragma unroll 4
+        for (int k4 = 0; k4 < 48; ++k4) {
+            uint4 wv = wp4[k4*576 + t];
+            float4 xv = *(const float4*)&sX[4*k4];
+            g0 += bflo(wv.x)*xv.x + bflo(wv.y)*xv.y + bflo(wv.z)*xv.z + bflo(wv.w)*xv.w;
+            g1 += bfhi(wv.x)*xv.x + bfhi(wv.y)*xv.y + bfhi(wv.z)*xv.z + bfhi(wv.w)*xv.w;
+        }
+        u64 ov = ((u64)(uint32_t)(STP + i) << 32)
+               | (u64)(f2bf(g0 + bv0) | (f2bf(g1 + bv1) << 16));
+        agstore(&PREcW[(size_t)(b*N_ + i)*G3 + t], ov);
         __syncthreads();
     }
 }
@@ -671,60 +542,55 @@
     const float* __restrict__ mw1, const float* __restrict__ mb1,
     const float* __restrict__ mw2, const float* __restrict__ mb2,
     float* __restrict__ Hcat, float* __restrict__ PREg,
-    float* __restrict__ WpreT, uint32_t* __restrict__ W4,
-    uint32_t* __restrict__ Wr4, uint32_t* __restrict__ Wp4w,
+    float* __restrict__ WpreT, uint32_t* __restrict__ Wc,
+    uint32_t* __restrict__ Wp,
     float* __restrict__ biasPre, float* __restrict__ gbx,
-    uint32_t* __restrict__ Hb, u64* __restrict__ MPs, u64* __restrict__ Kd,
-    u64* __restrict__ Hc, u64* __restrict__ PREc, u64* __restrict__ XQc,
+    u64* __restrict__ Hc, u64* __restrict__ PREc,
     u64* __restrict__ Fp, u64* __restrict__ Fd,
     float* __restrict__ out)
 {
-    __shared__ __align__(16) char smem[sizeof(ScanSm)];
+    __shared__ __align__(16) char smem[sizeof(SmemAll)];
     const int blk = blockIdx.x, t = threadIdx.x;
-    const int wgid = blk;
-    const int b = blk & 7, r12 = blk >> 3;
-    const int role = r12 >> 2, w = r12 & 3;
 
     for (int j = 0; j < 4; ++j) {
-        int idx = wgid * 576 + t + 55296 * j;
-        prepack_slice(idx, wr0, wr1, c_wih, c_whh, c_bih, c_bhh,
+        int idx = blk * 576 + t + 55296 * j;
+        prepack_slice(idx, c_wih, c_whh, c_bih, c_bhh,
                       p_wih, p_whh, p_bih, p_bhh,
-                      WpreT, W4, Wr4, Wp4w, biasPre, gbx);
-    }
-    flag_sync(Fp, wgid, t, SPK);
-
-    prologue(smem, wgid, t, features, fc1_w, fc1_b, WpreT, biasPre,
+                      WpreT, Wc, Wp, biasPre, gbx);
+    }
+    flag_sync(Fp, blk, t, SPK);
+
+    prologue(smem, blk, t, features, fc1_w, fc1_b, WpreT, biasPre,
              Hcat, PREg, Fp);
 
     float* As = out + 393216;
-    if (role == 0) {
-        scan_body<0>((ScanSm*)smem, b, w, t,
-            Hcat, Hcat + 192, PREg, adj, smask,
-            W4, Wr4, gbx, gatw,
-            Hb + (size_t)(b * NW + w) * KD * N_, MPs, Kd,
-            Hc, nullptr, nullptr, nullptr,
-            As + (size_t)b * (L_ * N_ * N_), 1);
+    if (blk < 8) {
+        const int b = blk;
+        scan_full<0>((ScanSm*)smem, b, t,
+            Hcat, Hcat + DH_, PREg, adj, smask,
+            Wc, wr0, wr1, gbx, gatw + DH_,
+            Hc, nullptr, nullptr,
+            As + (size_t)b * (2 * N_ * N_));
         __threadfence();
         __syncthreads();
-        if (t == 0) agstore(&Fd[b * 8 + w], packvs(0.f, SDN));
-    } else if (role == 2) {
-        scan_body<1>((ScanSm*)smem, b, w, t,
-            nullptr, Hcat + 384, nullptr, adj, smask,
-            W4 + NW * 27648, Wr4 + NW * 9216, gbx + 384, gatw + 384,
-            Hb + (size_t)(32 + b * NW + w) * KD * N_,
-            MPs + (size_t)8 * NW * DH_, Kd + 8 * NW,
-            nullptr, Hc, PREc, XQc,
-            As + (size_t)b * (L_ * N_ * N_) + N_ * N_, 30001);
+        if (t == 0) agstore(&Fd[b], packvs(0.f, SDN));
+    } else if (blk < 16) {
+        const int b = blk - 8;
+        worker_full((float*)smem, b, t, Wp, biasPre + G6, Hc, PREc);
+    } else if (blk < 24) {
+        const int b = blk - 16;
+        scan_full<1>((ScanSm*)smem, b, t,
+            nullptr, Hcat + 2 * DH_, nullptr, adj, smask,
+            Wc + 110592, wr0 + DH_ * DH_, wr1 + DH_ * DH_,
+            gbx + 384, gatw + 384 + DH_,
+            nullptr, Hc, PREc,
+            As + (size_t)b * (2 * N_ * N_) + N_ * N_);
         __threadfence();
         __syncthreads();
-        if (t == 0) agstore(&Fd[b * 8 + 4 + w], packvs(0.f, SDN));
-    } else {
-        worker_body((WorkSm*)smem, b, w, t,
-            Wp4w + (size_t)w * 27648, biasPre + G6, gatw + 384,
-            Hc, PREc, XQc);
-    }
-
-    mlp_tail(smem, wgid, t, Hcat, mw0, mb0, mw1, mb1, mw2, mb2, out, Fd);
+        if (t == 0) agstore(&Fd[8 + b], packvs(0.f, SDN));
+    }
+
+    mlp_tail(smem, blk, t, Hcat, mw0, mb0, mw1, mb1, mw2, mb2, out, Fd);
 }
 
 extern "C" void kernel_launch(void* const* d_in, const int* in_sizes, int n_in,
@@ -764,18 +630,13 @@
     };
     float* Hcat     = (float*)carve(2048ull * 576 * 4);
     float* PREg     = (float*)carve(2048ull * 1152 * 4);
-    float* WpreT    = (float*)carve(192ull * 1152 * 4);
-    uint32_t* W4    = (uint32_t*)carve(2ull * NW * 27648 * 4);
-    uint32_t* Wr4   = (uint32_t*)carve(2ull * NW * 9216 * 4);
-    uint32_t* Wp4w  = (uint32_t*)carve((size_t)NW * 27648 * 4);
-    float* biasPre  = (float*)carve(2ull * 1152 * 4);
-    float* gbx      = (float*)carve(2ull * 384 * 4);
-    uint32_t* Hb    = (uint32_t*)carve(64ull * KD * 256 * 4);
-    u64* MPs        = (u64*)carve(2ull * 8 * NW * DH_ * 8);
-    u64* Kd         = (u64*)carve(2ull * 8 * NW * 8);
-    u64* Hc         = (u64*)carve(8ull * 256 * NW * DS * 8);
-    u64* PREc       = (u64*)carve(8ull * 256 * NW * 144 * 8);
-    u64* XQc        = (u64*)carve(8ull * 256 * 8);
+    float* WpreT    = (float*)carve(221184ull * 4);
+    uint32_t* Wc    = (uint32_t*)carve(221184ull * 4);
+    uint32_t* Wp    = (uint32_t*)carve(110592ull * 4);
+    float* biasPre  = (float*)carve(2304ull * 4);
+    float* gbx      = (float*)carve(768ull * 4);
+    u64* Hc         = (u64*)carve(2048ull * 192 * 8);
+    u64* PREc       = (u64*)carve(2048ull * 576 * 8);
     u64* Fp         = (u64*)carve(288ull * 8);
     u64* Fd         = (u64*)carve(64ull * 8);
 
@@ -783,6 +644,6 @@
         features, fc1_w, fc1_b, adj, smask, gat_w,
         wr0, wr1, c_wih, c_whh, c_bih, c_bhh, p_wih, p_whh, p_bih, p_bhh,
         mw0, mb0, mw1, mb1, mw2, mb2,
-        Hcat, PREg, WpreT, W4, Wr4, Wp4w, biasPre, gbx,
-        Hb, MPs, Kd, Hc, PREc, XQc, Fp, Fd, out);
-}
+        Hcat, PREg, WpreT, Wc, Wp, biasPre, gbx,
+        Hc, PREc, Fp, Fd, out);
+}
```

Result: slower. 3.722 ms (+94.3%).
